# Kernel tuning notes

Measured on AMD Instinct MI355X. Metric: run time of the kernel, lower is better.

Reference implementation:

```python
import jax, jax.numpy as jnp
import numpy as np

DIM = 128; TIME_DIM = 256; HEADS = 8; WS = 4; GROUPS = 32
B = 8; H = 128; W = 128; EPS = 1e-5

def _rel_pos_index(ws):
    c = np.stack(np.meshgrid(np.arange(ws), np.arange(ws), indexing='ij')).reshape(2, -1)
    rel = (c[:, :, None] - c[:, None, :]).transpose(1, 2, 0)
    rel[:, :, 0] += ws - 1; rel[:, :, 1] += ws - 1
    rel[:, :, 0] *= 2 * ws - 1
    return jnp.asarray(rel.sum(-1))  # (ws*ws, ws*ws) int

REL_IDX = _rel_pos_index(WS)

def group_norm(x, w, b):
    Bx, C, Hx, Wx = x.shape
    xg = x.reshape(Bx, GROUPS, C // GROUPS, Hx, Wx)
    m = xg.mean((2, 3, 4), keepdims=True)
    v = xg.var((2, 3, 4), keepdims=True)
    x = ((xg - m) * jax.lax.rsqrt(v + EPS)).reshape(Bx, C, Hx, Wx)
    return x * w[None, :, None, None] + b[None, :, None, None]

def ada_gn(x, w, b, scale, shift):
    return group_norm(x, w, b) * (1.0 + scale[:, :, None, None]) + shift[:, :, None, None]

def time_mlp(t, w1, b1, w2, b2):
    h = jax.nn.silu(t @ w1.T + b1)
    out = h @ w2.T + b2
    scale, shift = jnp.split(out, 2, axis=-1)
    return scale, shift

def conv1x1(x, w, b):
    return jnp.einsum('bchw,oc->bohw', x, w) + b[None, :, None, None]

def window_attn(x, qkv_w, qkv_b, proj_w, proj_b, rel_bias):
    Bx, C, Hx, Wx = x.shape
    hd = C // HEADS
    nH, nW = Hx // WS, Wx // WS
    # partition into non-overlapping WSxWS windows -> (Nw, T, C)
    xw = x.transpose(0, 2, 3, 1).reshape(Bx, nH, WS, nW, WS, C)
    xw = xw.transpose(0, 1, 3, 2, 4, 5).reshape(Bx * nH * nW, WS * WS, C)
    qkv = xw @ qkv_w.T + qkv_b
    Nw, T, _ = qkv.shape
    qkv = qkv.reshape(Nw, T, 3, HEADS, hd).transpose(2, 0, 3, 1, 4)
    q, k, v = qkv[0], qkv[1], qkv[2]
    attn = jnp.einsum('whtd,whsd->whts', q, k) * (hd ** -0.5)
    bias = rel_bias[REL_IDX]  # (T, T, heads) gather from Swin rel-pos table
    attn = jax.nn.softmax(attn + bias.transpose(2, 0, 1)[None], axis=-1)
    out = jnp.einsum('whts,whsd->whtd', attn, v).transpose(0, 2, 1, 3).reshape(Nw, T, C)
    out = out @ proj_w.T + proj_b
    out = out.reshape(Bx, nH, nW, WS, WS, C).transpose(0, 1, 3, 2, 4, 5).reshape(Bx, Hx, Wx, C)
    return out.transpose(0, 3, 1, 2)

def reference(x, t_emb, gn1_w, gn1_b, t1_w1, t1_b1, t1_w2, t1_b2, spec_w, spec_b, mode_w,
              gn2_w, gn2_b, t2_w1, t2_b1, t2_w2, t2_b2, qkv_w, qkv_b, proj_w, proj_b, rel_bias,
              gn3_w, gn3_b, t3_w1, t3_b1, t3_w2, t3_b2, mlp_w1, mlp_b1, mlp_w2, mlp_b2,
              sb_gn_w, sb_gn_b, dw_w, dw_b, pw_w, pw_b):
    # --- AdaGN -> DCTSpectralConv -> SiLU -> residual ---
    s1, sh1 = time_mlp(t_emb, t1_w1, t1_b1, t1_w2, t1_b2)
    h = ada_gn(x, gn1_w, gn1_b, s1, sh1)
    h = h * jax.nn.sigmoid(mode_w)[None, :, None, None]  # per-mode weighting
    h = conv1x1(h, spec_w, spec_b)
    x = x + jax.nn.silu(h)
    # --- AdaGN -> windowed attention -> residual ---
    s2, sh2 = time_mlp(t_emb, t2_w1, t2_b1, t2_w2, t2_b2)
    h = ada_gn(x, gn2_w, gn2_b, s2, sh2)
    x = x + window_attn(h, qkv_w, qkv_b, proj_w, proj_b, rel_bias)
    # --- AdaGN -> ChannelMLP -> residual ---
    s3, sh3 = time_mlp(t_emb, t3_w1, t3_b1, t3_w2, t3_b2)
    h = ada_gn(x, gn3_w, gn3_b, s3, sh3)
    h = conv1x1(h, mlp_w1, mlp_b1)
    h = jax.nn.silu(h)
    h = conv1x1(h, mlp_w2, mlp_b2)
    x = x + h
    # --- SpatialBlock: GN -> depthwise 3x3 -> SiLU -> pointwise -> residual ---
    h = group_norm(x, sb_gn_w, sb_gn_b)
    h = jax.lax.conv_general_dilated(h, dw_w, (1, 1), 'SAME', feature_group_count=DIM,
                                     dimension_numbers=('NCHW', 'OIHW', 'NCHW'))
    h = h + dw_b[None, :, None, None]
    h = jax.nn.silu(h)
    h = conv1x1(h, pw_w, pw_b)
    return x + h


def setup_inputs() -> dict:
    key = jax.random.key(0)
    ks = jax.random.split(key, 24)
    r = lambda i, shape, s=1.0: jax.random.normal(ks[i], shape, dtype=jnp.float32) * s
    ones = lambda n: jnp.ones((n,), jnp.float32)
    zeros = lambda n: jnp.zeros((n,), jnp.float32)
    return {
        'x': r(0, (B, DIM, H, W)),
        't_emb': r(1, (B, TIME_DIM)),
        'gn1_w': ones(DIM), 'gn1_b': zeros(DIM),
        't1_w1': r(2, (DIM * 4, TIME_DIM), 0.02), 't1_b1': zeros(DIM * 4),
        't1_w2': r(3, (DIM * 2, DIM * 4), 0.02), 't1_b2': zeros(DIM * 2),
        'spec_w': r(4, (DIM, DIM), 0.05), 'spec_b': zeros(DIM),
        'mode_w': ones(DIM),
        'gn2_w': ones(DIM), 'gn2_b': zeros(DIM),
        't2_w1': r(5, (DIM * 4, TIME_DIM), 0.02), 't2_b1': zeros(DIM * 4),
        't2_w2': r(6, (DIM * 2, DIM * 4), 0.02), 't2_b2': zeros(DIM * 2),
        'qkv_w': r(7, (3 * DIM, DIM), 0.05), 'qkv_b': zeros(3 * DIM),
        'proj_w': r(8, (DIM, DIM), 0.05), 'proj_b': zeros(DIM),
        'rel_bias': r(9, ((2 * WS - 1) ** 2, HEADS), 0.02),
        'gn3_w': ones(DIM), 'gn3_b': zeros(DIM),
        't3_w1': r(10, (DIM * 4, TIME_DIM), 0.02), 't3_b1': zeros(DIM * 4),
        't3_w2': r(11, (DIM * 2, DIM * 4), 0.02), 't3_b2': zeros(DIM * 2),
        'mlp_w1': r(12, (DIM * 4, DIM), 0.05), 'mlp_b1': zeros(DIM * 4),
        'mlp_w2': r(13, (DIM, DIM * 4), 0.05), 'mlp_b2': zeros(DIM),
        'sb_gn_w': ones(DIM), 'sb_gn_b': zeros(DIM),
        'dw_w': r(14, (DIM, 1, 3, 3), 0.1), 'dw_b': zeros(DIM),
        'pw_w': r(15, (DIM, DIM), 0.05), 'pw_b': zeros(DIM),
    }
```

## Files before the change

### kernel.cpp

```cpp
#include <hip/hip_runtime.h>

#define PTOT 131072
#define IMGP 16384
#define BATCH 8
#define EPSV 1e-5f

typedef short bf16x8 __attribute__((ext_vector_type(8)));
typedef float f32x4 __attribute__((ext_vector_type(4)));

__device__ __forceinline__ float bf2f(unsigned short u){
  union { unsigned int i; float f; } v; v.i = ((unsigned int)u) << 16; return v.f;
}
__device__ __forceinline__ unsigned short f2bf(float f){
  union { float f; unsigned int i; } v; v.f = f;
  unsigned int r = v.i + 0x7FFFu + ((v.i >> 16) & 1u);
  return (unsigned short)(r >> 16);
}
__device__ __forceinline__ unsigned int pk2(float a, float b){
  return (unsigned int)f2bf(a) | ((unsigned int)f2bf(b) << 16);
}
__device__ __forceinline__ float sigmoidf_(float x){ return 1.f/(1.f + __expf(-x)); }

__device__ __forceinline__ void ld16bf(const unsigned short* p, float* f){
  uint4 u0 = *(const uint4*)p;
  uint4 u1 = *(const uint4*)(p+8);
  f[0]=bf2f((unsigned short)u0.x); f[1]=bf2f((unsigned short)(u0.x>>16));
  f[2]=bf2f((unsigned short)u0.y); f[3]=bf2f((unsigned short)(u0.y>>16));
  f[4]=bf2f((unsigned short)u0.z); f[5]=bf2f((unsigned short)(u0.z>>16));
  f[6]=bf2f((unsigned short)u0.w); f[7]=bf2f((unsigned short)(u0.w>>16));
  f[8]=bf2f((unsigned short)u1.x); f[9]=bf2f((unsigned short)(u1.x>>16));
  f[10]=bf2f((unsigned short)u1.y); f[11]=bf2f((unsigned short)(u1.y>>16));
  f[12]=bf2f((unsigned short)u1.z); f[13]=bf2f((unsigned short)(u1.z>>16));
  f[14]=bf2f((unsigned short)u1.w); f[15]=bf2f((unsigned short)(u1.w>>16));
}

__global__ __launch_bounds__(256) void k_prep(
    const float* __restrict__ a0, const float* __restrict__ a1,
    const float* __restrict__ a2, const float* __restrict__ a3,
    const float* __restrict__ a4, const float* __restrict__ a5,
    unsigned short* __restrict__ dst)
{
  int i = blockIdx.x*256 + threadIdx.x;
  if (i >= 229376) return;
  float v;
  if (i < 16384) v = a0[i];
  else if (i < 65536) v = a1[i-16384];
  else if (i < 81920) v = a2[i-65536];
  else if (i < 147456) v = a3[i-81920];
  else if (i < 212992) v = a4[i-147456];
  else v = a5[i-212992];
  dst[i] = f2bf(v);
}

__global__ __launch_bounds__(256) void k_time_mlp(
    const float* __restrict__ temb,
    const float* __restrict__ w1a, const float* __restrict__ b1a,
    const float* __restrict__ w2a, const float* __restrict__ b2a,
    const float* __restrict__ w1b, const float* __restrict__ b1b,
    const float* __restrict__ w2b, const float* __restrict__ b2b,
    const float* __restrict__ w1c, const float* __restrict__ b1c,
    const float* __restrict__ w2c, const float* __restrict__ b2c,
    float* __restrict__ scsh)
{
  int b = blockIdx.x, s = blockIdx.y, t = threadIdx.x;
  const float* w1 = (s==0)? w1a : ((s==1)? w1b : w1c);
  const float* b1 = (s==0)? b1a : ((s==1)? b1b : b1c);
  const float* w2 = (s==0)? w2a : ((s==1)? w2b : w2c);
  const float* b2 = (s==0)? b2a : ((s==1)? b2b : b2c);
  __shared__ float te[256];
  __shared__ float hb[512];
  te[t] = temb[b*256 + t];
  __syncthreads();
  for (int k = t; k < 512; k += 256){
    float acc = b1[k];
    const float* wr = w1 + (size_t)k*256;
    for (int j = 0; j < 256; j += 4){
      float4 w = *(const float4*)(wr + j);
      acc += w.x*te[j] + w.y*te[j+1] + w.z*te[j+2] + w.w*te[j+3];
    }
    hb[k] = acc * sigmoidf_(acc);
  }
  __syncthreads();
  {
    float acc = b2[t];
    const float* wr = w2 + (size_t)t*512;
    for (int j = 0; j < 512; j += 4){
      float4 w = *(const float4*)(wr + j);
      acc += w.x*hb[j] + w.y*hb[j+1] + w.z*hb[j+2] + w.w*hb[j+3];
    }
    scsh[(size_t)(s*BATCH + b)*256 + t] = acc;
  }
}

__global__ __launch_bounds__(256) void k_pre(
    const float* __restrict__ x0, float* __restrict__ X0T, float* __restrict__ SG1)
{
  __shared__ __align__(16) float T[64*136];
  __shared__ float sgS[32], sgSS[32];
  int t = threadIdx.x;
  int p0 = blockIdx.x << 6;
  int b = p0 >> 14;
  int win0 = (p0 >> 4) & 1023;
  int wh = win0 >> 5, ww0 = win0 & 31;
  if (t < 32){ sgS[t]=0.f; sgSS[t]=0.f; }
  int q = t & 3;
  int cb = t >> 2;
  #pragma unroll
  for (int ci = 0; ci < 2; ++ci){
    int c = cb + ci*64;
    const float* src = x0 + ((size_t)(b*128 + c))*IMGP + (wh*4)*128 + ww0*4 + q*4;
    #pragma unroll
    for (int ty = 0; ty < 4; ++ty){
      float4 v = *(const float4*)(src + ty*128);
      T[(q*16 + ty*4 + 0)*136 + c] = v.x;
      T[(q*16 + ty*4 + 1)*136 + c] = v.y;
      T[(q*16 + ty*4 + 2)*136 + c] = v.z;
      T[(q*16 + ty*4 + 3)*136 + c] = v.w;
    }
  }
  __syncthreads();
  {
    int px = t >> 2, c0 = (t & 3) << 5;
    float* dst = X0T + ((size_t)(p0+px))*128 + c0;
    const float* src = T + px*136 + c0;
    #pragma unroll
    for (int gi = 0; gi < 8; ++gi){
      float4 v = *(const float4*)(src + gi*4);
      *(float4*)(dst + gi*4) = v;
      atomicAdd(&sgS[(c0>>2)+gi],  v.x+v.y+v.z+v.w);
      atomicAdd(&sgSS[(c0>>2)+gi], v.x*v.x+v.y*v.y+v.z*v.z+v.w*v.w);
    }
  }
  __syncthreads();
  if (t < 32){
    atomicAdd(&SG1[(b*32+t)*2],   sgS[t]);
    atomicAdd(&SG1[(b*32+t)*2+1], sgSS[t]);
  }
}

__global__ __launch_bounds__(256) void k_s1(
    const float* __restrict__ X0T,
    const float* __restrict__ SG1, float* __restrict__ SG2,
    const unsigned short* __restrict__ Wbf, const float* __restrict__ bias,
    const float* __restrict__ gnw, const float* __restrict__ gnb,
    const float* __restrict__ scsh, const float* __restrict__ modew,
    float* __restrict__ XR)
{
  __shared__ __align__(16) unsigned short Bs[64*136];
  __shared__ __align__(16) char UN[64*136*4];
  __shared__ float An[128], Bn[128];
  __shared__ float sgS[32], sgSS[32];
  unsigned short* As = (unsigned short*)UN;
  float* OT = (float*)UN;
  int t = threadIdx.x;
  int p0 = blockIdx.x << 6;
  int b = p0 >> 14;
  if (t < 128){
    int g = t >> 2;
    float S = SG1[(b*32+g)*2], SS = SG1[(b*32+g)*2+1];
    float m = S*(1.f/65536.f);
    float r = rsqrtf(SS*(1.f/65536.f) - m*m + EPSV);
    float sc = 1.f + scsh[b*256 + t];
    float sh = scsh[b*256 + 128 + t];
    float a = r*gnw[t]*sc;
    float bb = (gnb[t] - m*r*gnw[t])*sc + sh;
    float sg = sigmoidf_(modew[t]); a *= sg; bb *= sg;
    An[t] = a; Bn[t] = bb;
  }
  if (t < 32){ sgS[t]=0.f; sgSS[t]=0.f; }
  __syncthreads();
  {
    int px = t >> 2, c0 = (t & 3) << 5;
    const float* src = X0T + ((size_t)(p0+px))*128 + c0;
    unsigned short* dst = Bs + px*136 + c0;
    #pragma unroll
    for (int j = 0; j < 4; ++j){
      float4 v0 = *(const float4*)(src + j*8);
      float4 v1 = *(const float4*)(src + j*8 + 4);
      int c = c0 + j*8;
      uint4 w;
      w.x = pk2(fmaf(v0.x,An[c+0],Bn[c+0]), fmaf(v0.y,An[c+1],Bn[c+1]));
      w.y = pk2(fmaf(v0.z,An[c+2],Bn[c+2]), fmaf(v0.w,An[c+3],Bn[c+3]));
      w.z = pk2(fmaf(v1.x,An[c+4],Bn[c+4]), fmaf(v1.y,An[c+5],Bn[c+5]));
      w.w = pk2(fmaf(v1.z,An[c+6],Bn[c+6]), fmaf(v1.w,An[c+7],Bn[c+7]));
      *(uint4*)(dst + j*8) = w;
    }
  }
  f32x4 acc[2][4];
  #pragma unroll
  for (int i=0;i<2;++i)
    #pragma unroll
    for (int j=0;j<4;++j){ f32x4 z={0.f,0.f,0.f,0.f}; acc[i][j]=z; }
  int lane = t & 63, wv = t >> 6, quad = lane >> 4, l15 = lane & 15;
  for (int kc = 0; kc < 2; ++kc){
    __syncthreads();
    {
      int o = t >> 1, k0 = (t & 1) << 5;
      const unsigned short* src = Wbf + o*128 + kc*64 + k0;
      unsigned short* dst = As + o*72 + k0;
      #pragma unroll
      for (int j = 0; j < 4; ++j) *(uint4*)(dst + j*8) = *(const uint4*)(src + j*8);
    }
    __syncthreads();
    #pragma unroll
    for (int s = 0; s < 2; ++s){
      bf16x8 af[2], bfv[4];
      #pragma unroll
      for (int i=0;i<2;++i) af[i] = *(const bf16x8*)(As + (wv*32 + i*16 + l15)*72 + s*32 + quad*8);
      #pragma unroll
      for (int j=0;j<4;++j) bfv[j] = *(const bf16x8*)(Bs + (j*16 + l15)*136 + kc*64 + s*32 + quad*8);
      #pragma unroll
      for (int i=0;i<2;++i)
        #pragma unroll
        for (int j=0;j<4;++j)
          acc[i][j] = __builtin_amdgcn_mfma_f32_16x16x32_bf16(af[i], bfv[j], acc[i][j], 0,0,0);
    }
  }
  __syncthreads();
  #pragma unroll
  for (int i = 0; i < 2; ++i){
    int o = wv*32 + i*16 + (quad<<2);
    float4 bv = *(const float4*)(bias + o);
    #pragma unroll
    for (int j = 0; j < 4; ++j){
      int px = j*16 + l15;
      float v0=acc[i][j][0]+bv.x, v1=acc[i][j][1]+bv.y, v2=acc[i][j][2]+bv.z, v3=acc[i][j][3]+bv.w;
      v0*=sigmoidf_(v0); v1*=sigmoidf_(v1); v2*=sigmoidf_(v2); v3*=sigmoidf_(v3);
      float4 rv = *(const float4*)(X0T + ((size_t)(p0+px))*128 + o);
      v0+=rv.x; v1+=rv.y; v2+=rv.z; v3+=rv.w;
      *(float4*)(OT + px*136 + o) = make_float4(v0,v1,v2,v3);
    }
  }
  __syncthreads();
  {
    int px = t >> 2, c0 = (t & 3) << 5;
    float* dst = XR + ((size_t)(p0+px))*128 + c0;
    const float* src = OT + px*136 + c0;
    #pragma unroll
    for (int gi = 0; gi < 8; ++gi){
      float4 v = *(const float4*)(src + gi*4);
      *(float4*)(dst + gi*4) = v;
      atomicAdd(&sgS[(c0>>2)+gi],  v.x+v.y+v.z+v.w);
      atomicAdd(&sgSS[(c0>>2)+gi], v.x*v.x+v.y*v.y+v.z*v.z+v.w*v.w);
    }
  }
  __syncthreads();
  if (t < 32){
    atomicAdd(&SG2[(b*32+t)*2],   sgS[t]);
    atomicAdd(&SG2[(b*32+t)*2+1], sgSS[t]);
  }
}

__global__ __launch_bounds__(256) void k_s2(
    float* __restrict__ XR,
    const float* __restrict__ SG2, float* __restrict__ SG3,
    const unsigned short* __restrict__ Wqkv, const float* __restrict__ bqkv,
    const unsigned short* __restrict__ Wproj, const float* __restrict__ bproj,
    const float* __restrict__ relb,
    const float* __restrict__ gnw, const float* __restrict__ gnb,
    const float* __restrict__ scsh)
{
  __shared__ __align__(16) unsigned short Bs[32*136];
  __shared__ __align__(16) unsigned short QB[32*136];
  __shared__ __align__(16) unsigned short KB[32*136];
  __shared__ __align__(16) unsigned short VB[32*136];
  __shared__ __align__(16) char UN[18432];
  __shared__ float An[128], Bn[128];
  __shared__ float relbs[392];
  __shared__ float sgS[32], sgSS[32];
  unsigned short* As = (unsigned short*)UN;
  float* OT = (float*)UN;
  int t = threadIdx.x;
  int p0 = blockIdx.x << 5;
  int b = p0 >> 14;
  if (t < 128){
    int g = t >> 2;
    float S = SG2[(b*32+g)*2], SS = SG2[(b*32+g)*2+1];
    float m = S*(1.f/65536.f);
    float r = rsqrtf(SS*(1.f/65536.f) - m*m + EPSV);
    float sc = 1.f + scsh[b*256 + t];
    float sh = scsh[b*256 + 128 + t];
    An[t] = r*gnw[t]*sc;
    Bn[t] = (gnb[t] - m*r*gnw[t])*sc + sh;
  }
  for (int j = t; j < 392; j += 256) relbs[j] = relb[j];
  if (t < 32){ sgS[t]=0.f; sgSS[t]=0.f; }
  __syncthreads();
  {
    int px = t >> 3, c0 = (t & 7) << 4;
    const float* src = XR + ((size_t)(p0+px))*128 + c0;
    unsigned short* dst = Bs + px*136 + c0;
    #pragma unroll
    for (int j = 0; j < 2; ++j){
      float4 v0 = *(const float4*)(src + j*8);
      float4 v1 = *(const float4*)(src + j*8 + 4);
      int c = c0 + j*8;
      uint4 w;
      w.x = pk2(fmaf(v0.x,An[c+0],Bn[c+0]), fmaf(v0.y,An[c+1],Bn[c+1]));
      w.y = pk2(fmaf(v0.z,An[c+2],Bn[c+2]), fmaf(v0.w,An[c+3],Bn[c+3]));
      w.z = pk2(fmaf(v1.x,An[c+4],Bn[c+4]), fmaf(v1.y,An[c+5],Bn[c+5]));
      w.w = pk2(fmaf(v1.z,An[c+6],Bn[c+6]), fmaf(v1.w,An[c+7],Bn[c+7]));
      *(uint4*)(dst + j*8) = w;
    }
  }
  int lane = t & 63, wv = t >> 6, quad = lane >> 4, l15 = lane & 15;
  unsigned short* bufs[3] = {QB, KB, VB};
  for (int s = 0; s < 3; ++s){
    f32x4 acc[2][2];
    #pragma unroll
    for (int i=0;i<2;++i)
      #pragma unroll
      for (int j=0;j<2;++j){ f32x4 z={0.f,0.f,0.f,0.f}; acc[i][j]=z; }
    for (int kc = 0; kc < 2; ++kc){
      __syncthreads();
      {
        int o = t >> 1, k0 = (t & 1) << 5;
        const unsigned short* src = Wqkv + (size_t)(s*128+o)*128 + kc*64 + k0;
        unsigned short* dst = As + o*72 + k0;
        #pragma unroll
        for (int j = 0; j < 4; ++j) *(uint4*)(dst + j*8) = *(const uint4*)(src + j*8);
      }
      __syncthreads();
      #pragma unroll
      for (int ks = 0; ks < 2; ++ks){
        bf16x8 af[2], bfv[2];
        #pragma unroll
        for (int i=0;i<2;++i) af[i] = *(const bf16x8*)(As + (wv*32 + i*16 + l15)*72 + ks*32 + quad*8);
        #pragma unroll
        for (int j=0;j<2;++j) bfv[j] = *(const bf16x8*)(Bs + (j*16 + l15)*136 + kc*64 + ks*32 + quad*8);
        #pragma unroll
        for (int i=0;i<2;++i)
          #pragma unroll
          for (int j=0;j<2;++j)
            acc[i][j] = __builtin_amdgcn_mfma_f32_16x16x32_bf16(af[i], bfv[j], acc[i][j], 0,0,0);
      }
    }
    unsigned short* dstb = bufs[s];
    #pragma unroll
    for (int i = 0; i < 2; ++i){
      int o = wv*32 + i*16 + (quad<<2);
      float4 bv = *(const float4*)(bqkv + s*128 + o);
      #pragma unroll
      for (int j = 0; j < 2; ++j){
        int px = j*16 + l15;
        *(unsigned int*)(dstb + px*136 + o)     = pk2(acc[i][j][0]+bv.x, acc[i][j][1]+bv.y);
        *(unsigned int*)(dstb + px*136 + o + 2) = pk2(acc[i][j][2]+bv.z, acc[i][j][3]+bv.w);
      }
    }
  }
  __syncthreads();
  {
    int win = t >> 7, head = (t >> 4) & 7, tq = t & 15;
    float qv[16];
    ld16bf(QB + (win*16+tq)*136 + head*16, qv);
    float pr[16]; float mx = -1e30f;
    int ty = tq >> 2, tx = tq & 3;
    #pragma unroll
    for (int s16 = 0; s16 < 16; ++s16){
      float kv[16];
      ld16bf(KB + (win*16+s16)*136 + head*16, kv);
      float dot = 0.f;
      #pragma unroll
      for (int d = 0; d < 16; ++d) dot = fmaf(qv[d], kv[d], dot);
      int idx = (ty-(s16>>2)+3)*7 + (tx-(s16&3)+3);
      pr[s16] = dot*0.25f + relbs[idx*8 + head];
      mx = fmaxf(mx, pr[s16]);
    }
    float sum = 0.f;
    #pragma unroll
    for (int s16 = 0; s16 < 16; ++s16){ pr[s16] = __expf(pr[s16]-mx); sum += pr[s16]; }
    float inv = 1.f/sum;
    #pragma unroll
    for (int s16 = 0; s16 < 16; ++s16) pr[s16] *= inv;
    __syncthreads();
    float ov[16];
    #pragma unroll
    for (int d = 0; d < 16; ++d) ov[d] = 0.f;
    #pragma unroll
    for (int s16 = 0; s16 < 16; ++s16){
      float vv[16];
      ld16bf(VB + (win*16+s16)*136 + head*16, vv);
      #pragma unroll
      for (int d = 0; d < 16; ++d) ov[d] = fmaf(pr[s16], vv[d], ov[d]);
    }
    unsigned short* dst = QB + (win*16+tq)*136 + head*16;
    uint4 w0, w1;
    w0.x = pk2(ov[0],ov[1]);   w0.y = pk2(ov[2],ov[3]);
    w0.z = pk2(ov[4],ov[5]);   w0.w = pk2(ov[6],ov[7]);
    w1.x = pk2(ov[8],ov[9]);   w1.y = pk2(ov[10],ov[11]);
    w1.z = pk2(ov[12],ov[13]); w1.w = pk2(ov[14],ov[15]);
    *(uint4*)dst = w0;
    *(uint4*)(dst+8) = w1;
  }
  f32x4 acc[2][2];
  #pragma unroll
  for (int i=0;i<2;++i)
    #pragma unroll
    for (int j=0;j<2;++j){ f32x4 z={0.f,0.f,0.f,0.f}; acc[i][j]=z; }
  for (int kc = 0; kc < 2; ++kc){
    __syncthreads();
    {
      int o = t >> 1, k0 = (t & 1) << 5;
      const unsigned short* src = Wproj + (size_t)o*128 + kc*64 + k0;
      unsigned short* dst = As + o*72 + k0;
      #pragma unroll
      for (int j = 0; j < 4; ++j) *(uint4*)(dst + j*8) = *(const uint4*)(src + j*8);
    }
    __syncthreads();
    #pragma unroll
    for (int ks = 0; ks < 2; ++ks){
      bf16x8 af[2], bfv[2];
      #pragma unroll
      for (int i=0;i<2;++i) af[i] = *(const bf16x8*)(As + (wv*32 + i*16 + l15)*72 + ks*32 + quad*8);
      #pragma unroll
      for (int j=0;j<2;++j) bfv[j] = *(const bf16x8*)(QB + (j*16 + l15)*136 + kc*64 + ks*32 + quad*8);
      #pragma unroll
      for (int i=0;i<2;++i)
        #pragma unroll
        for (int j=0;j<2;++j)
          acc[i][j] = __builtin_amdgcn_mfma_f32_16x16x32_bf16(af[i], bfv[j], acc[i][j], 0,0,0);
    }
  }
  __syncthreads();
  #pragma unroll
  for (int i = 0; i < 2; ++i){
    int o = wv*32 + i*16 + (quad<<2);
    float4 bv = *(const float4*)(bproj + o);
    #pragma unroll
    for (int j = 0; j < 2; ++j){
      int px = j*16 + l15;
      float v0=acc[i][j][0]+bv.x, v1=acc[i][j][1]+bv.y, v2=acc[i][j][2]+bv.z, v3=acc[i][j][3]+bv.w;
      float4 rv = *(const float4*)(XR + ((size_t)(p0+px))*128 + o);
      v0+=rv.x; v1+=rv.y; v2+=rv.z; v3+=rv.w;
      *(float4*)(OT + px*136 + o) = make_float4(v0,v1,v2,v3);
    }
  }
  __syncthreads();
  {
    int px = t >> 3, c0 = (t & 7) << 4;
    float* dst = XR + ((size_t)(p0+px))*128 + c0;
    const float* src = OT + px*136 + c0;
    #pragma unroll
    for (int gi = 0; gi < 4; ++gi){
      float4 v = *(const float4*)(src + gi*4);
      *(float4*)(dst + gi*4) = v;
      atomicAdd(&sgS[(c0>>2)+gi],  v.x+v.y+v.z+v.w);
      atomicAdd(&sgSS[(c0>>2)+gi], v.x*v.x+v.y*v.y+v.z*v.z+v.w*v.w);
    }
  }
  __syncthreads();
  if (t < 32){
    atomicAdd(&SG3[(b*32+t)*2],   sgS[t]);
    atomicAdd(&SG3[(b*32+t)*2+1], sgSS[t]);
  }
}

__global__ __launch_bounds__(256) void k_s3(
    float* __restrict__ XR,
    const float* __restrict__ SG3, float* __restrict__ SG4,
    const unsigned short* __restrict__ W1, const float* __restrict__ b1,
    const unsigned short* __restrict__ W2, const float* __restrict__ b2,
    const float* __restrict__ gnw, const float* __restrict__ gnb,
    const float* __restrict__ scsh)
{
  __shared__ __align__(16) unsigned short Xs[64*136];
  __shared__ __align__(16) char UN[45056];
  __shared__ float An[128], Bn[128];
  __shared__ float sgS[32], sgSS[32];
  unsigned short* As1 = (unsigned short*)UN;
  unsigned short* Hs  = (unsigned short*)(UN + 17408);
  unsigned short* As2 = (unsigned short*)(UN + 26624);
  float* OT = (float*)UN;
  int t = threadIdx.x;
  int p0 = blockIdx.x << 6;
  int b = p0 >> 14;
  if (t < 128){
    int g = t >> 2;
    float S = SG3[(b*32+g)*2], SS = SG3[(b*32+g)*2+1];
    float m = S*(1.f/65536.f);
    float r = rsqrtf(SS*(1.f/65536.f) - m*m + EPSV);
    float sc = 1.f + scsh[b*256 + t];
    float sh = scsh[b*256 + 128 + t];
    An[t] = r*gnw[t]*sc;
    Bn[t] = (gnb[t] - m*r*gnw[t])*sc + sh;
  }
  if (t < 32){ sgS[t]=0.f; sgSS[t]=0.f; }
  __syncthreads();
  {
    int px = t >> 2, c0 = (t & 3) << 5;
    const float* src = XR + ((size_t)(p0+px))*128 + c0;
    unsigned short* dst = Xs + px*136 + c0;
    #pragma unroll
    for (int j = 0; j < 4; ++j){
      float4 v0 = *(const float4*)(src + j*8);
      float4 v1 = *(const float4*)(src + j*8 + 4);
      int c = c0 + j*8;
      uint4 w;
      w.x = pk2(fmaf(v0.x,An[c+0],Bn[c+0]), fmaf(v0.y,An[c+1],Bn[c+1]));
      w.y = pk2(fmaf(v0.z,An[c+2],Bn[c+2]), fmaf(v0.w,An[c+3],Bn[c+3]));
      w.z = pk2(fmaf(v1.x,An[c+4],Bn[c+4]), fmaf(v1.y,An[c+5],Bn[c+5]));
      w.w = pk2(fmaf(v1.z,An[c+6],Bn[c+6]), fmaf(v1.w,An[c+7],Bn[c+7]));
      *(uint4*)(dst + j*8) = w;
    }
  }
  int lane = t & 63, wv = t >> 6, quad = lane >> 4, l15 = lane & 15;
  f32x4 acc2[2][4];
  #pragma unroll
  for (int i=0;i<2;++i)
    #pragma unroll
    for (int j=0;j<4;++j){ f32x4 z={0.f,0.f,0.f,0.f}; acc2[i][j]=z; }
  for (int hc = 0; hc < 8; ++hc){
    __syncthreads();
    {
      int hr = t >> 2, k0 = (t & 3) << 5;
      const unsigned short* src = W1 + (size_t)(hc*64+hr)*128 + k0;
      unsigned short* dst = As1 + hr*136 + k0;
      #pragma unroll
      for (int j = 0; j < 4; ++j) *(uint4*)(dst + j*8) = *(const uint4*)(src + j*8);
    }
    {
      int o = t >> 1, k0 = (t & 1) << 5;
      const unsigned short* src = W2 + (size_t)o*512 + hc*64 + k0;
      unsigned short* dst = As2 + o*72 + k0;
      #pragma unroll
      for (int j = 0; j < 4; ++j) *(uint4*)(dst + j*8) = *(const uint4*)(src + j*8);
    }
    __syncthreads();
    {
      int hb = (wv & 1) << 5, pxb = (wv >> 1) << 5;
      f32x4 a1[2][2];
      #pragma unroll
      for (int i=0;i<2;++i)
        #pragma unroll
        for (int j=0;j<2;++j){ f32x4 z={0.f,0.f,0.f,0.f}; a1[i][j]=z; }
      #pragma unroll
      for (int s = 0; s < 4; ++s){
        bf16x8 af[2], bfv[2];
        #pragma unroll
        for (int i=0;i<2;++i) af[i] = *(const bf16x8*)(As1 + (hb + i*16 + l15)*136 + s*32 + quad*8);
        #pragma unroll
        for (int j=0;j<2;++j) bfv[j] = *(const bf16x8*)(Xs + (pxb + j*16 + l15)*136 + s*32 + quad*8);
        #pragma unroll
        for (int i=0;i<2;++i)
          #pragma unroll
          for (int j=0;j<2;++j)
            a1[i][j] = __builtin_amdgcn_mfma_f32_16x16x32_bf16(af[i], bfv[j], a1[i][j], 0,0,0);
      }
      #pragma unroll
      for (int i = 0; i < 2; ++i){
        int hl = hb + i*16 + (quad<<2);
        float4 bv = *(const float4*)(b1 + hc*64 + hl);
        #pragma unroll
        for (int j = 0; j < 2; ++j){
          int px = pxb + j*16 + l15;
          float v0=a1[i][j][0]+bv.x, v1=a1[i][j][1]+bv.y, v2=a1[i][j][2]+bv.z, v3=a1[i][j][3]+bv.w;
          v0*=sigmoidf_(v0); v1*=sigmoidf_(v1); v2*=sigmoidf_(v2); v3*=sigmoidf_(v3);
          *(unsigned int*)(Hs + px*72 + hl)     = pk2(v0, v1);
          *(unsigned int*)(Hs + px*72 + hl + 2) = pk2(v2, v3);
        }
      }
    }
    __syncthreads();
    {
      int ob = wv << 5;
      #pragma unroll
      for (int s = 0; s < 2; ++s){
        bf16x8 af[2], bfv[4];
        #pragma unroll
        for (int i=0;i<2;++i) af[i] = *(const bf16x8*)(As2 + (ob + i*16 + l15)*72 + s*32 + quad*8);
        #pragma unroll
        for (int j=0;j<4;++j) bfv[j] = *(const bf16x8*)(Hs + (j*16 + l15)*72 + s*32 + quad*8);
        #pragma unroll
        for (int i=0;i<2;++i)
          #pragma unroll
          for (int j=0;j<4;++j)
            acc2[i][j] = __builtin_amdgcn_mfma_f32_16x16x32_bf16(af[i], bfv[j], acc2[i][j], 0,0,0);
      }
    }
  }
  __syncthreads();
  #pragma unroll
  for (int i = 0; i < 2; ++i){
    int o = (wv<<5) + i*16 + (quad<<2);
    float4 bv = *(const float4*)(b2 + o);
    #pragma unroll
    for (int j = 0; j < 4; ++j){
      int px = j*16 + l15;
      float v0=acc2[i][j][0]+bv.x, v1=acc2[i][j][1]+bv.y, v2=acc2[i][j][2]+bv.z, v3=acc2[i][j][3]+bv.w;
      float4 rv = *(const float4*)(XR + ((size_t)(p0+px))*128 + o);
      v0+=rv.x; v1+=rv.y; v2+=rv.z; v3+=rv.w;
      *(float4*)(OT + px*136 + o) = make_float4(v0,v1,v2,v3);
    }
  }
  __syncthreads();
  {
    int px = t >> 2, c0 = (t & 3) << 5;
    float* dst = XR + ((size_t)(p0+px))*128 + c0;
    const float* src = OT + px*136 + c0;
    #pragma unroll
    for (int gi = 0; gi < 8; ++gi){
      float4 v = *(const float4*)(src + gi*4);
      *(float4*)(dst + gi*4) = v;
      atomicAdd(&sgS[(c0>>2)+gi],  v.x+v.y+v.z+v.w);
      atomicAdd(&sgSS[(c0>>2)+gi], v.x*v.x+v.y*v.y+v.z*v.z+v.w*v.w);
    }
  }
  __syncthreads();
  if (t < 32){
    atomicAdd(&SG4[(b*32+t)*2],   sgS[t]);
    atomicAdd(&SG4[(b*32+t)*2+1], sgSS[t]);
  }
}

__global__ __launch_bounds__(256) void k_dw(
    const float* __restrict__ XR, const float* __restrict__ SG4,
    const float* __restrict__ gnw, const float* __restrict__ gnb,
    const float* __restrict__ dww, const float* __restrict__ dwb,
    unsigned short* __restrict__ DWO)
{
  __shared__ float wt[9*128];
  __shared__ float An[128], Bn[128];
  int t = threadIdx.x;
  int p0 = blockIdx.x << 6;
  int b = p0 >> 14;
  int win0 = (p0 >> 4) & 1023;
  int wh = win0 >> 5, ww0 = win0 & 31;
  if (t < 128){
    int g = t >> 2;
    float S = SG4[(b*32+g)*2], SS = SG4[(b*32+g)*2+1];
    float m = S*(1.f/65536.f);
    float r = rsqrtf(SS*(1.f/65536.f) - m*m + EPSV);
    float A = r*gnw[t];
    An[t] = A;
    Bn[t] = gnb[t] - m*A;
  }
  for (int j = t; j < 1152; j += 256){ int c = j/9, tap = j%9; wt[tap*128 + c] = dww[j]; }
  __syncthreads();
  int pxl = t & 63, ck = t >> 6;
  int c0 = ck << 5;
  int wloc = pxl >> 4, ty = (pxl >> 2) & 3, tx = pxl & 3;
  int h = wh*4 + ty, w = (ww0 + wloc)*4 + tx;
  float acc[32];
  #pragma unroll
  for (int j = 0; j < 8; ++j){
    float4 bv = *(const float4*)(dwb + c0 + j*4);
    acc[j*4+0]=bv.x; acc[j*4+1]=bv.y; acc[j*4+2]=bv.z; acc[j*4+3]=bv.w;
  }
  #pragma unroll
  for (int dy = -1; dy <= 1; ++dy){
    int hh = h + dy;
    if (hh < 0 || hh > 127) continue;
    #pragma unroll
    for (int dx = -1; dx <= 1; ++dx){
      int wn = w + dx;
      if (wn < 0 || wn > 127) continue;
      int pn = b*IMGP + ((hh>>2)*32 + (wn>>2))*16 + (hh&3)*4 + (wn&3);
      const float* xp = XR + (size_t)pn*128 + c0;
      const float* wp = wt + ((dy+1)*3 + (dx+1))*128 + c0;
      #pragma unroll
      for (int j = 0; j < 8; ++j){
        float4 xv = *(const float4*)(xp + j*4);
        float4 wv = *(const float4*)(wp + j*4);
        int c = c0 + j*4;
        acc[j*4+0] = fmaf(wv.x, fmaf(An[c+0], xv.x, Bn[c+0]), acc[j*4+0]);
        acc[j*4+1] = fmaf(wv.y, fmaf(An[c+1], xv.y, Bn[c+1]), acc[j*4+1]);
        acc[j*4+2] = fmaf(wv.z, fmaf(An[c+2], xv.z, Bn[c+2]), acc[j*4+2]);
        acc[j*4+3] = fmaf(wv.w, fmaf(An[c+3], xv.w, Bn[c+3]), acc[j*4+3]);
      }
    }
  }
  unsigned short* dst = DWO + ((size_t)(p0+pxl))*128 + c0;
  #pragma unroll
  for (int j = 0; j < 4; ++j){
    float v0 = acc[j*8+0], v1 = acc[j*8+1], v2 = acc[j*8+2], v3 = acc[j*8+3];
    float v4 = acc[j*8+4], v5 = acc[j*8+5], v6 = acc[j*8+6], v7 = acc[j*8+7];
    v0*=sigmoidf_(v0); v1*=sigmoidf_(v1); v2*=sigmoidf_(v2); v3*=sigmoidf_(v3);
    v4*=sigmoidf_(v4); v5*=sigmoidf_(v5); v6*=sigmoidf_(v6); v7*=sigmoidf_(v7);
    uint4 wq;
    wq.x = pk2(v0,v1); wq.y = pk2(v2,v3); wq.z = pk2(v4,v5); wq.w = pk2(v6,v7);
    *(uint4*)(dst + j*8) = wq;
  }
}

__global__ __launch_bounds__(256) void k_s4(
    const unsigned short* __restrict__ DWO,
    const unsigned short* __restrict__ Wbf, const float* __restrict__ bias,
    const float* __restrict__ XR, float* __restrict__ out)
{
  __shared__ __align__(16) unsigned short Bs[64*136];
  __shared__ __align__(16) char UN[64*136*4];
  unsigned short* As = (unsigned short*)UN;
  float* OT = (float*)UN;
  int t = threadIdx.x;
  int p0 = blockIdx.x << 6;
  int b = p0 >> 14;
  int win0 = (p0 >> 4) & 1023;
  int wh = win0 >> 5, ww0 = win0 & 31;
  {
    int px = t >> 2, c0 = (t & 3) << 5;
    const unsigned short* src = DWO + ((size_t)(p0+px))*128 + c0;
    unsigned short* dst = Bs + px*136 + c0;
    #pragma unroll
    for (int j = 0; j < 4; ++j) *(uint4*)(dst + j*8) = *(const uint4*)(src + j*8);
  }
  f32x4 acc[2][4];
  #pragma unroll
  for (int i=0;i<2;++i)
    #pragma unroll
    for (int j=0;j<4;++j){ f32x4 z={0.f,0.f,0.f,0.f}; acc[i][j]=z; }
  int lane = t & 63, wv = t >> 6, quad = lane >> 4, l15 = lane & 15;
  for (int kc = 0; kc < 2; ++kc){
    __syncthreads();
    {
      int o = t >> 1, k0 = (t & 1) << 5;
      const unsigned short* src = Wbf + (size_t)o*128 + kc*64 + k0;
      unsigned short* dst = As + o*72 + k0;
      #pragma unroll
      for (int j = 0; j < 4; ++j) *(uint4*)(dst + j*8) = *(const uint4*)(src + j*8);
    }
    __syncthreads();
    #pragma unroll
    for (int s = 0; s < 2; ++s){
      bf16x8 af[2], bfv[4];
      #pragma unroll
      for (int i=0;i<2;++i) af[i] = *(const bf16x8*)(As + (wv*32 + i*16 + l15)*72 + s*32 + quad*8);
      #pragma unroll
      for (int j=0;j<4;++j) bfv[j] = *(const bf16x8*)(Bs + (j*16 + l15)*136 + kc*64 + s*32 + quad*8);
      #pragma unroll
      for (int i=0;i<2;++i)
        #pragma unroll
        for (int j=0;j<4;++j)
          acc[i][j] = __builtin_amdgcn_mfma_f32_16x16x32_bf16(af[i], bfv[j], acc[i][j], 0,0,0);
    }
  }
  __syncthreads();
  #pragma unroll
  for (int i = 0; i < 2; ++i){
    int o = (wv<<5) + i*16 + (quad<<2);
    float4 bv = *(const float4*)(bias + o);
    #pragma unroll
    for (int j = 0; j < 4; ++j){
      int px = j*16 + l15;
      float v0=acc[i][j][0]+bv.x, v1=acc[i][j][1]+bv.y, v2=acc[i][j][2]+bv.z, v3=acc[i][j][3]+bv.w;
      float4 rv = *(const float4*)(XR + ((size_t)(p0+px))*128 + o);
      v0+=rv.x; v1+=rv.y; v2+=rv.z; v3+=rv.w;
      *(float4*)(OT + px*136 + o) = make_float4(v0,v1,v2,v3);
    }
  }
  __syncthreads();
  #pragma unroll
  for (int it = 0; it < 2; ++it){
    int item = t + (it << 8);
    int c = item >> 2, ty = item & 3;
    float vbuf[16];
    #pragma unroll
    for (int wl = 0; wl < 4; ++wl)
      #pragma unroll
      for (int tx = 0; tx < 4; ++tx)
        vbuf[wl*4+tx] = OT[(wl*16 + ty*4 + tx)*136 + c];
    float* dst = out + ((size_t)(b*128 + c))*IMGP + (wh*4+ty)*128 + ww0*4;
    #pragma unroll
    for (int j = 0; j < 4; ++j)
      *(float4*)(dst + j*4) = make_float4(vbuf[j*4], vbuf[j*4+1], vbuf[j*4+2], vbuf[j*4+3]);
  }
}

extern "C" void kernel_launch(void* const* d_in, const int* in_sizes, int n_in,
                              void* d_out, int out_size, void* d_ws, size_t ws_size,
                              hipStream_t stream)
{
  const float* x0   = (const float*)d_in[0];
  const float* temb = (const float*)d_in[1];
  const float* gn1w = (const float*)d_in[2];
  const float* gn1b = (const float*)d_in[3];
  const float* t1w1 = (const float*)d_in[4];
  const float* t1b1 = (const float*)d_in[5];
  const float* t1w2 = (const float*)d_in[6];
  const float* t1b2 = (const float*)d_in[7];
  const float* specw= (const float*)d_in[8];
  const float* specb= (const float*)d_in[9];
  const float* modew= (const float*)d_in[10];
  const float* gn2w = (const float*)d_in[11];
  const float* gn2b = (const float*)d_in[12];
  const float* t2w1 = (const float*)d_in[13];
  const float* t2b1 = (const float*)d_in[14];
  const float* t2w2 = (const float*)d_in[15];
  const float* t2b2 = (const float*)d_in[16];
  const float* qkvw = (const float*)d_in[17];
  const float* qkvb = (const float*)d_in[18];
  const float* projw= (const float*)d_in[19];
  const float* projb= (const float*)d_in[20];
  const float* relb = (const float*)d_in[21];
  const float* gn3w = (const float*)d_in[22];
  const float* gn3b = (const float*)d_in[23];
  const float* t3w1 = (const float*)d_in[24];
  const float* t3b1 = (const float*)d_in[25];
  const float* t3w2 = (const float*)d_in[26];
  const float* t3b2 = (const float*)d_in[27];
  const float* mlpw1= (const float*)d_in[28];
  const float* mlpb1= (const float*)d_in[29];
  const float* mlpw2= (const float*)d_in[30];
  const float* mlpb2= (const float*)d_in[31];
  const float* sbgnw= (const float*)d_in[32];
  const float* sbgnb= (const float*)d_in[33];
  const float* dww  = (const float*)d_in[34];
  const float* dwb  = (const float*)d_in[35];
  const float* pww  = (const float*)d_in[36];
  const float* pwb  = (const float*)d_in[37];
  float* out = (float*)d_out;

  char* ws = (char*)d_ws;
  float* SC  = (float*)ws;
  float* SG  = (float*)(ws + 32768);
  float* SG1 = SG, *SG2 = SG+512, *SG3 = SG+1024, *SG4 = SG+1536;
  unsigned short* WBF = (unsigned short*)(ws + 65536);
  unsigned short* Wspec = WBF;
  unsigned short* Wqkv  = WBF + 16384;
  unsigned short* Wproj = WBF + 65536;
  unsigned short* Wmlp1 = WBF + 81920;
  unsigned short* Wmlp2 = WBF + 147456;
  unsigned short* Wpw   = WBF + 212992;
  float* X0T = (float*)(ws + (1u<<20));
  float* XR  = (float*)(ws + (1u<<20) + ((size_t)64<<20));
  unsigned short* DWO = (unsigned short*)(ws + (1u<<20) + ((size_t)128<<20));

  hipMemsetAsync(SG, 0, 4*512*sizeof(float), stream);

  k_prep<<<896, 256, 0, stream>>>(specw, qkvw, projw, mlpw1, mlpw2, pww, WBF);
  k_time_mlp<<<dim3(8,3), 256, 0, stream>>>(temb,
      t1w1,t1b1,t1w2,t1b2, t2w1,t2b1,t2w2,t2b2, t3w1,t3b1,t3w2,t3b2, SC);
  k_pre<<<2048, 256, 0, stream>>>(x0, X0T, SG1);
  k_s1<<<2048, 256, 0, stream>>>(X0T, SG1, SG2, Wspec, specb,
      gn1w, gn1b, SC + 0, modew, XR);
  k_s2<<<4096, 256, 0, stream>>>(XR, SG2, SG3, Wqkv, qkvb, Wproj, projb,
      relb, gn2w, gn2b, SC + 2048);
  k_s3<<<2048, 256, 0, stream>>>(XR, SG3, SG4, Wmlp1, mlpb1, Wmlp2, mlpb2,
      gn3w, gn3b, SC + 4096);
  k_dw<<<2048, 256, 0, stream>>>(XR, SG4, sbgnw, sbgnb, dww, dwb, DWO);
  k_s4<<<2048, 256, 0, stream>>>(DWO, Wpw, pwb, XR, out);
}
```

Baseline: 810.5 us.

## Store intermediates in bf16, split attention into QKV GEMM and attention-proj kernels

Intermediate activations (transposed input, residual stream, depthwise output) are now stored as bf16 instead of fp32, which halves global memory traffic between stages. The combined window-attention kernel is split into a separate QKV GEMM kernel and an attention-plus-projection kernel that works on spatial strips. The GEMM tiles grow to 128 pixels per block with a 4x4 MFMA tile per wave. Pixel ordering changes from window-major to row-major, so the final output store is coalesced. The cost is lower precision in the residual stream and an extra QKV round trip through global memory.

```diff
diff --git a/kernel.cpp b/kernel.cpp
--- a/kernel.cpp
+++ b/kernel.cpp
@@ -1,6 +1,5 @@
 #include <hip/hip_runtime.h>
 
-#define PTOT 131072
 #define IMGP 16384
 #define BATCH 8
 #define EPSV 1e-5f
@@ -21,17 +20,19 @@
 }
 __device__ __forceinline__ float sigmoidf_(float x){ return 1.f/(1.f + __expf(-x)); }
 
-__device__ __forceinline__ void ld16bf(const unsigned short* p, float* f){
-  uint4 u0 = *(const uint4*)p;
-  uint4 u1 = *(const uint4*)(p+8);
-  f[0]=bf2f((unsigned short)u0.x); f[1]=bf2f((unsigned short)(u0.x>>16));
-  f[2]=bf2f((unsigned short)u0.y); f[3]=bf2f((unsigned short)(u0.y>>16));
-  f[4]=bf2f((unsigned short)u0.z); f[5]=bf2f((unsigned short)(u0.z>>16));
-  f[6]=bf2f((unsigned short)u0.w); f[7]=bf2f((unsigned short)(u0.w>>16));
-  f[8]=bf2f((unsigned short)u1.x); f[9]=bf2f((unsigned short)(u1.x>>16));
-  f[10]=bf2f((unsigned short)u1.y); f[11]=bf2f((unsigned short)(u1.y>>16));
-  f[12]=bf2f((unsigned short)u1.z); f[13]=bf2f((unsigned short)(u1.z>>16));
-  f[14]=bf2f((unsigned short)u1.w); f[15]=bf2f((unsigned short)(u1.w>>16));
+__device__ __forceinline__ void ub8(uint4 u, float* f){
+  f[0]=bf2f((unsigned short)(u.x&0xffff)); f[1]=bf2f((unsigned short)(u.x>>16));
+  f[2]=bf2f((unsigned short)(u.y&0xffff)); f[3]=bf2f((unsigned short)(u.y>>16));
+  f[4]=bf2f((unsigned short)(u.z&0xffff)); f[5]=bf2f((unsigned short)(u.z>>16));
+  f[6]=bf2f((unsigned short)(u.w&0xffff)); f[7]=bf2f((unsigned short)(u.w>>16));
+}
+__device__ __forceinline__ uint4 pb8(const float* f){
+  uint4 r; r.x = pk2(f[0],f[1]); r.y = pk2(f[2],f[3]);
+  r.z = pk2(f[4],f[5]); r.w = pk2(f[6],f[7]); return r;
+}
+__device__ __forceinline__ void ld16lds(const unsigned short* p, float* f){
+  uint4 u0 = *(const uint4*)p; uint4 u1 = *(const uint4*)(p+8);
+  ub8(u0, f); ub8(u1, f+8);
 }
 
 __global__ __launch_bounds__(256) void k_prep(
@@ -52,7 +53,7 @@
   dst[i] = f2bf(v);
 }
 
-__global__ __launch_bounds__(256) void k_time_mlp(
+__global__ __launch_bounds__(256) void k_tmlp(
     const float* __restrict__ temb,
     const float* __restrict__ w1a, const float* __restrict__ b1a,
     const float* __restrict__ w2a, const float* __restrict__ b2a,
@@ -93,43 +94,41 @@
 }
 
 __global__ __launch_bounds__(256) void k_pre(
-    const float* __restrict__ x0, float* __restrict__ X0T, float* __restrict__ SG1)
-{
-  __shared__ __align__(16) float T[64*136];
+    const float* __restrict__ x0, unsigned short* __restrict__ X0b, float* __restrict__ SG1)
+{
+  __shared__ __align__(16) unsigned short T[64*136];
   __shared__ float sgS[32], sgSS[32];
   int t = threadIdx.x;
   int p0 = blockIdx.x << 6;
   int b = p0 >> 14;
-  int win0 = (p0 >> 4) & 1023;
-  int wh = win0 >> 5, ww0 = win0 & 31;
+  int hw0 = p0 & 16383;
   if (t < 32){ sgS[t]=0.f; sgSS[t]=0.f; }
-  int q = t & 3;
-  int cb = t >> 2;
-  #pragma unroll
-  for (int ci = 0; ci < 2; ++ci){
-    int c = cb + ci*64;
-    const float* src = x0 + ((size_t)(b*128 + c))*IMGP + (wh*4)*128 + ww0*4 + q*4;
-    #pragma unroll
-    for (int ty = 0; ty < 4; ++ty){
-      float4 v = *(const float4*)(src + ty*128);
-      T[(q*16 + ty*4 + 0)*136 + c] = v.x;
-      T[(q*16 + ty*4 + 1)*136 + c] = v.y;
-      T[(q*16 + ty*4 + 2)*136 + c] = v.z;
-      T[(q*16 + ty*4 + 3)*136 + c] = v.w;
-    }
+  __syncthreads();
+  {
+    int c = t >> 1, q = t & 1;
+    const float* src = x0 + (size_t)(b*128 + c)*IMGP + hw0 + q*32;
+    float s = 0.f, ss = 0.f;
+    #pragma unroll
+    for (int i = 0; i < 8; ++i){
+      float4 v = *(const float4*)(src + i*4);
+      int px = q*32 + i*4;
+      T[(px+0)*136 + c] = f2bf(v.x);
+      T[(px+1)*136 + c] = f2bf(v.y);
+      T[(px+2)*136 + c] = f2bf(v.z);
+      T[(px+3)*136 + c] = f2bf(v.w);
+      s  += v.x + v.y + v.z + v.w;
+      ss += v.x*v.x + v.y*v.y + v.z*v.z + v.w*v.w;
+    }
+    atomicAdd(&sgS[c>>2], s);
+    atomicAdd(&sgSS[c>>2], ss);
   }
   __syncthreads();
   {
     int px = t >> 2, c0 = (t & 3) << 5;
-    float* dst = X0T + ((size_t)(p0+px))*128 + c0;
-    const float* src = T + px*136 + c0;
-    #pragma unroll
-    for (int gi = 0; gi < 8; ++gi){
-      float4 v = *(const float4*)(src + gi*4);
-      *(float4*)(dst + gi*4) = v;
-      atomicAdd(&sgS[(c0>>2)+gi],  v.x+v.y+v.z+v.w);
-      atomicAdd(&sgSS[(c0>>2)+gi], v.x*v.x+v.y*v.y+v.z*v.z+v.w*v.w);
-    }
+    unsigned short* dst = X0b + (size_t)(p0+px)*128 + c0;
+    const unsigned short* srcT = T + px*136 + c0;
+    #pragma unroll
+    for (int g = 0; g < 4; ++g) *(uint4*)(dst + g*8) = *(const uint4*)(srcT + g*8);
   }
   __syncthreads();
   if (t < 32){
@@ -139,21 +138,21 @@
 }
 
 __global__ __launch_bounds__(256) void k_s1(
-    const float* __restrict__ X0T,
+    const unsigned short* __restrict__ X0b,
     const float* __restrict__ SG1, float* __restrict__ SG2,
     const unsigned short* __restrict__ Wbf, const float* __restrict__ bias,
     const float* __restrict__ gnw, const float* __restrict__ gnb,
     const float* __restrict__ scsh, const float* __restrict__ modew,
-    float* __restrict__ XR)
-{
-  __shared__ __align__(16) unsigned short Bs[64*136];
-  __shared__ __align__(16) char UN[64*136*4];
+    unsigned short* __restrict__ XRb)
+{
+  __shared__ __align__(16) char UN[36864];
   __shared__ float An[128], Bn[128];
   __shared__ float sgS[32], sgSS[32];
   unsigned short* As = (unsigned short*)UN;
-  float* OT = (float*)UN;
+  unsigned short* Bs = (unsigned short*)(UN + 18432);
+  unsigned short* OT = (unsigned short*)UN;
   int t = threadIdx.x;
-  int p0 = blockIdx.x << 6;
+  int p0 = blockIdx.x << 7;
   int b = p0 >> 14;
   if (t < 128){
     int g = t >> 2;
@@ -169,48 +168,45 @@
   }
   if (t < 32){ sgS[t]=0.f; sgSS[t]=0.f; }
   __syncthreads();
-  {
-    int px = t >> 2, c0 = (t & 3) << 5;
-    const float* src = X0T + ((size_t)(p0+px))*128 + c0;
-    unsigned short* dst = Bs + px*136 + c0;
-    #pragma unroll
-    for (int j = 0; j < 4; ++j){
-      float4 v0 = *(const float4*)(src + j*8);
-      float4 v1 = *(const float4*)(src + j*8 + 4);
-      int c = c0 + j*8;
-      uint4 w;
-      w.x = pk2(fmaf(v0.x,An[c+0],Bn[c+0]), fmaf(v0.y,An[c+1],Bn[c+1]));
-      w.y = pk2(fmaf(v0.z,An[c+2],Bn[c+2]), fmaf(v0.w,An[c+3],Bn[c+3]));
-      w.z = pk2(fmaf(v1.x,An[c+4],Bn[c+4]), fmaf(v1.y,An[c+5],Bn[c+5]));
-      w.w = pk2(fmaf(v1.z,An[c+6],Bn[c+6]), fmaf(v1.w,An[c+7],Bn[c+7]));
-      *(uint4*)(dst + j*8) = w;
-    }
-  }
-  f32x4 acc[2][4];
-  #pragma unroll
-  for (int i=0;i<2;++i)
+  int lane = t & 63, wv = t >> 6, quad = lane >> 4, l15 = lane & 15;
+  int wo = (wv & 1) << 6, wp = (wv >> 1) << 6;
+  f32x4 acc[4][4];
+  #pragma unroll
+  for (int i=0;i<4;++i)
     #pragma unroll
     for (int j=0;j<4;++j){ f32x4 z={0.f,0.f,0.f,0.f}; acc[i][j]=z; }
-  int lane = t & 63, wv = t >> 6, quad = lane >> 4, l15 = lane & 15;
   for (int kc = 0; kc < 2; ++kc){
-    __syncthreads();
-    {
-      int o = t >> 1, k0 = (t & 1) << 5;
-      const unsigned short* src = Wbf + o*128 + kc*64 + k0;
-      unsigned short* dst = As + o*72 + k0;
+    if (kc) __syncthreads();
+    { int o = t >> 1, kh = (t & 1) << 5;
+      const unsigned short* src = Wbf + o*128 + kc*64 + kh;
+      unsigned short* dst = As + o*72 + kh;
       #pragma unroll
       for (int j = 0; j < 4; ++j) *(uint4*)(dst + j*8) = *(const uint4*)(src + j*8);
     }
+    { int px = t >> 1, kh = (t & 1) << 5;
+      const unsigned short* src = X0b + (size_t)(p0+px)*128 + kc*64 + kh;
+      unsigned short* dst = Bs + px*72 + kh;
+      #pragma unroll
+      for (int j = 0; j < 4; ++j){
+        uint4 u = *(const uint4*)(src + j*8);
+        float f[8], g[8];
+        ub8(u, f);
+        int c = kc*64 + kh + j*8;
+        #pragma unroll
+        for (int e = 0; e < 8; ++e) g[e] = fmaf(f[e], An[c+e], Bn[c+e]);
+        *(uint4*)(dst + j*8) = pb8(g);
+      }
+    }
     __syncthreads();
     #pragma unroll
     for (int s = 0; s < 2; ++s){
-      bf16x8 af[2], bfv[4];
-      #pragma unroll
-      for (int i=0;i<2;++i) af[i] = *(const bf16x8*)(As + (wv*32 + i*16 + l15)*72 + s*32 + quad*8);
-      #pragma unroll
-      for (int j=0;j<4;++j) bfv[j] = *(const bf16x8*)(Bs + (j*16 + l15)*136 + kc*64 + s*32 + quad*8);
-      #pragma unroll
-      for (int i=0;i<2;++i)
+      bf16x8 af[4], bfv[4];
+      #pragma unroll
+      for (int i=0;i<4;++i) af[i]  = *(const bf16x8*)(As + (wo+i*16+l15)*72 + s*32 + quad*8);
+      #pragma unroll
+      for (int j=0;j<4;++j) bfv[j] = *(const bf16x8*)(Bs + (wp+j*16+l15)*72 + s*32 + quad*8);
+      #pragma unroll
+      for (int i=0;i<4;++i)
         #pragma unroll
         for (int j=0;j<4;++j)
           acc[i][j] = __builtin_amdgcn_mfma_f32_16x16x32_bf16(af[i], bfv[j], acc[i][j], 0,0,0);
@@ -218,30 +214,38 @@
   }
   __syncthreads();
   #pragma unroll
-  for (int i = 0; i < 2; ++i){
-    int o = wv*32 + i*16 + (quad<<2);
+  for (int i = 0; i < 4; ++i){
+    int o = wo + i*16 + (quad<<2);
     float4 bv = *(const float4*)(bias + o);
     #pragma unroll
     for (int j = 0; j < 4; ++j){
-      int px = j*16 + l15;
+      int px = wp + j*16 + l15;
       float v0=acc[i][j][0]+bv.x, v1=acc[i][j][1]+bv.y, v2=acc[i][j][2]+bv.z, v3=acc[i][j][3]+bv.w;
       v0*=sigmoidf_(v0); v1*=sigmoidf_(v1); v2*=sigmoidf_(v2); v3*=sigmoidf_(v3);
-      float4 rv = *(const float4*)(X0T + ((size_t)(p0+px))*128 + o);
-      v0+=rv.x; v1+=rv.y; v2+=rv.z; v3+=rv.w;
-      *(float4*)(OT + px*136 + o) = make_float4(v0,v1,v2,v3);
+      uint2 w; w.x = pk2(v0,v1); w.y = pk2(v2,v3);
+      *(uint2*)(OT + px*136 + o) = w;
     }
   }
   __syncthreads();
   {
-    int px = t >> 2, c0 = (t & 3) << 5;
-    float* dst = XR + ((size_t)(p0+px))*128 + c0;
-    const float* src = OT + px*136 + c0;
-    #pragma unroll
-    for (int gi = 0; gi < 8; ++gi){
-      float4 v = *(const float4*)(src + gi*4);
-      *(float4*)(dst + gi*4) = v;
-      atomicAdd(&sgS[(c0>>2)+gi],  v.x+v.y+v.z+v.w);
-      atomicAdd(&sgSS[(c0>>2)+gi], v.x*v.x+v.y*v.y+v.z*v.z+v.w*v.w);
+    int px = t >> 1, c0 = (t & 1) << 6;
+    const unsigned short* rsrc = X0b + (size_t)(p0+px)*128 + c0;
+    unsigned short* dst = XRb + (size_t)(p0+px)*128 + c0;
+    #pragma unroll
+    for (int g = 0; g < 8; ++g){
+      uint4 hu = *(const uint4*)(OT + px*136 + c0 + g*8);
+      uint4 ru = *(const uint4*)(rsrc + g*8);
+      float hf[8], rf[8], v[8];
+      ub8(hu, hf); ub8(ru, rf);
+      #pragma unroll
+      for (int e = 0; e < 8; ++e) v[e] = hf[e] + rf[e];
+      float slo = v[0]+v[1]+v[2]+v[3], shi = v[4]+v[5]+v[6]+v[7];
+      float qlo = v[0]*v[0]+v[1]*v[1]+v[2]*v[2]+v[3]*v[3];
+      float qhi = v[4]*v[4]+v[5]*v[5]+v[6]*v[6]+v[7]*v[7];
+      int gb = (c0 + g*8) >> 2;
+      atomicAdd(&sgS[gb], slo);  atomicAdd(&sgS[gb+1], shi);
+      atomicAdd(&sgSS[gb], qlo); atomicAdd(&sgSS[gb+1], qhi);
+      *(uint4*)(dst + g*8) = pb8(v);
     }
   }
   __syncthreads();
@@ -251,28 +255,23 @@
   }
 }
 
-__global__ __launch_bounds__(256) void k_s2(
-    float* __restrict__ XR,
-    const float* __restrict__ SG2, float* __restrict__ SG3,
-    const unsigned short* __restrict__ Wqkv, const float* __restrict__ bqkv,
-    const unsigned short* __restrict__ Wproj, const float* __restrict__ bproj,
-    const float* __restrict__ relb,
+__global__ __launch_bounds__(256) void k_qkv(
+    const unsigned short* __restrict__ XRb,
+    const float* __restrict__ SG2,
+    const unsigned short* __restrict__ Wq, const float* __restrict__ bq,
     const float* __restrict__ gnw, const float* __restrict__ gnb,
-    const float* __restrict__ scsh)
-{
-  __shared__ __align__(16) unsigned short Bs[32*136];
-  __shared__ __align__(16) unsigned short QB[32*136];
-  __shared__ __align__(16) unsigned short KB[32*136];
-  __shared__ __align__(16) unsigned short VB[32*136];
-  __shared__ __align__(16) char UN[18432];
+    const float* __restrict__ scsh,
+    unsigned short* __restrict__ QKV)
+{
+  __shared__ __align__(16) char UN[36864];
   __shared__ float An[128], Bn[128];
-  __shared__ float relbs[392];
-  __shared__ float sgS[32], sgSS[32];
   unsigned short* As = (unsigned short*)UN;
-  float* OT = (float*)UN;
+  unsigned short* Bs = (unsigned short*)(UN + 18432);
+  unsigned short* OT = (unsigned short*)UN;
   int t = threadIdx.x;
-  int p0 = blockIdx.x << 5;
+  int p0 = blockIdx.x << 7;
   int b = p0 >> 14;
+  int sel = blockIdx.y;
   if (t < 128){
     int g = t >> 2;
     float S = SG2[(b*32+g)*2], SS = SG2[(b*32+g)*2+1];
@@ -283,169 +282,216 @@
     An[t] = r*gnw[t]*sc;
     Bn[t] = (gnb[t] - m*r*gnw[t])*sc + sh;
   }
+  __syncthreads();
+  int lane = t & 63, wv = t >> 6, quad = lane >> 4, l15 = lane & 15;
+  int wo = (wv & 1) << 6, wp = (wv >> 1) << 6;
+  f32x4 acc[4][4];
+  #pragma unroll
+  for (int i=0;i<4;++i)
+    #pragma unroll
+    for (int j=0;j<4;++j){ f32x4 z={0.f,0.f,0.f,0.f}; acc[i][j]=z; }
+  for (int kc = 0; kc < 2; ++kc){
+    if (kc) __syncthreads();
+    { int o = t >> 1, kh = (t & 1) << 5;
+      const unsigned short* src = Wq + (size_t)sel*16384 + o*128 + kc*64 + kh;
+      unsigned short* dst = As + o*72 + kh;
+      #pragma unroll
+      for (int j = 0; j < 4; ++j) *(uint4*)(dst + j*8) = *(const uint4*)(src + j*8);
+    }
+    { int px = t >> 1, kh = (t & 1) << 5;
+      const unsigned short* src = XRb + (size_t)(p0+px)*128 + kc*64 + kh;
+      unsigned short* dst = Bs + px*72 + kh;
+      #pragma unroll
+      for (int j = 0; j < 4; ++j){
+        uint4 u = *(const uint4*)(src + j*8);
+        float f[8], g[8];
+        ub8(u, f);
+        int c = kc*64 + kh + j*8;
+        #pragma unroll
+        for (int e = 0; e < 8; ++e) g[e] = fmaf(f[e], An[c+e], Bn[c+e]);
+        *(uint4*)(dst + j*8) = pb8(g);
+      }
+    }
+    __syncthreads();
+    #pragma unroll
+    for (int s = 0; s < 2; ++s){
+      bf16x8 af[4], bfv[4];
+      #pragma unroll
+      for (int i=0;i<4;++i) af[i]  = *(const bf16x8*)(As + (wo+i*16+l15)*72 + s*32 + quad*8);
+      #pragma unroll
+      for (int j=0;j<4;++j) bfv[j] = *(const bf16x8*)(Bs + (wp+j*16+l15)*72 + s*32 + quad*8);
+      #pragma unroll
+      for (int i=0;i<4;++i)
+        #pragma unroll
+        for (int j=0;j<4;++j)
+          acc[i][j] = __builtin_amdgcn_mfma_f32_16x16x32_bf16(af[i], bfv[j], acc[i][j], 0,0,0);
+    }
+  }
+  __syncthreads();
+  #pragma unroll
+  for (int i = 0; i < 4; ++i){
+    int o = wo + i*16 + (quad<<2);
+    float4 bv = *(const float4*)(bq + sel*128 + o);
+    #pragma unroll
+    for (int j = 0; j < 4; ++j){
+      int px = wp + j*16 + l15;
+      uint2 w; w.x = pk2(acc[i][j][0]+bv.x, acc[i][j][1]+bv.y);
+      w.y = pk2(acc[i][j][2]+bv.z, acc[i][j][3]+bv.w);
+      *(uint2*)(OT + px*136 + o) = w;
+    }
+  }
+  __syncthreads();
+  {
+    int px = t >> 1, og = (t & 1) << 6;
+    unsigned short* dst = QKV + (size_t)(p0+px)*384 + (sel << 7) + og;
+    const unsigned short* src = OT + px*136 + og;
+    #pragma unroll
+    for (int g = 0; g < 8; ++g) *(uint4*)(dst + g*8) = *(const uint4*)(src + g*8);
+  }
+}
+
+__global__ __launch_bounds__(256) void k_ap(
+    const unsigned short* __restrict__ QKV,
+    const unsigned short* __restrict__ Wproj, const float* __restrict__ bproj,
+    const float* __restrict__ relb,
+    unsigned short* __restrict__ XRb, float* __restrict__ SG3)
+{
+  __shared__ __align__(16) unsigned short AOb[128*136];
+  __shared__ __align__(16) unsigned short UNQ[12288];
+  __shared__ float relbs[392];
+  __shared__ float sgS[32], sgSS[32];
+  unsigned short* QKVs = UNQ;
+  unsigned short* As = UNQ;
+  int t = threadIdx.x;
+  int blk = blockIdx.x;
+  int b = blk >> 7;
+  int rem = blk & 127;
+  int h0 = (rem >> 2) << 2;
+  int w0 = (rem & 3) << 5;
+  int baseP = b*IMGP + h0*128 + w0;
   for (int j = t; j < 392; j += 256) relbs[j] = relb[j];
   if (t < 32){ sgS[t]=0.f; sgSS[t]=0.f; }
+  for (int hb = 0; hb < 8; hb += 2){
+    __syncthreads();
+    #pragma unroll
+    for (int pass = 0; pass < 6; ++pass){
+      int u = t + (pass << 8);
+      int sel = u >> 9;
+      int r = u & 511;
+      int hp = r >> 8;
+      int pxh = r & 255;
+      int pxl = pxh >> 1;
+      int dh = (pxh & 1) << 3;
+      int pg = baseP + ((pxl >> 5) << 7) + (pxl & 31);
+      *(uint4*)(QKVs + (((sel*2+hp) << 7) + pxl)*16 + dh) =
+        *(const uint4*)(QKV + (size_t)pg*384 + (sel << 7) + ((hb+hp) << 4) + dh);
+    }
+    __syncthreads();
+    {
+      int hp = t >> 7, win = (t >> 4) & 7, tq = t & 15;
+      int head = hb + hp;
+      int ty = tq >> 2, tx = tq & 3;
+      int pq = (ty << 5) + (win << 2) + tx;
+      float qv[16];
+      ld16lds(QKVs + ((hp << 7) + pq)*16, qv);
+      float pr[16]; float mx = -1e30f;
+      #pragma unroll
+      for (int s = 0; s < 16; ++s){
+        int ps = ((s >> 2) << 5) + (win << 2) + (s & 3);
+        float kv[16];
+        ld16lds(QKVs + (((2+hp) << 7) + ps)*16, kv);
+        float dot = 0.f;
+        #pragma unroll
+        for (int d = 0; d < 16; ++d) dot = fmaf(qv[d], kv[d], dot);
+        int idx = (ty-(s>>2)+3)*7 + (tx-(s&3)+3);
+        pr[s] = dot*0.25f + relbs[idx*8 + head];
+        mx = fmaxf(mx, pr[s]);
+      }
+      float sum = 0.f;
+      #pragma unroll
+      for (int s = 0; s < 16; ++s){ pr[s] = __expf(pr[s]-mx); sum += pr[s]; }
+      float inv = 1.f/sum;
+      float ov[16];
+      #pragma unroll
+      for (int d = 0; d < 16; ++d) ov[d] = 0.f;
+      #pragma unroll
+      for (int s = 0; s < 16; ++s){
+        int ps = ((s >> 2) << 5) + (win << 2) + (s & 3);
+        float vv[16];
+        ld16lds(QKVs + (((4+hp) << 7) + ps)*16, vv);
+        #pragma unroll
+        for (int d = 0; d < 16; ++d) ov[d] = fmaf(pr[s], vv[d], ov[d]);
+      }
+      #pragma unroll
+      for (int d = 0; d < 16; ++d) ov[d] *= inv;
+      unsigned short* dst = AOb + pq*136 + (head << 4);
+      *(uint4*)dst     = pb8(ov);
+      *(uint4*)(dst+8) = pb8(ov+8);
+    }
+  }
+  int lane = t & 63, wv = t >> 6, quad = lane >> 4, l15 = lane & 15;
+  int wo = (wv & 1) << 6, wp = (wv >> 1) << 6;
+  f32x4 acc[4][4];
+  #pragma unroll
+  for (int i=0;i<4;++i)
+    #pragma unroll
+    for (int j=0;j<4;++j){ f32x4 z={0.f,0.f,0.f,0.f}; acc[i][j]=z; }
+  for (int kc = 0; kc < 2; ++kc){
+    __syncthreads();
+    { int o = t >> 1, kh = (t & 1) << 5;
+      const unsigned short* src = Wproj + o*128 + kc*64 + kh;
+      unsigned short* dst = As + o*72 + kh;
+      #pragma unroll
+      for (int j = 0; j < 4; ++j) *(uint4*)(dst + j*8) = *(const uint4*)(src + j*8);
+    }
+    __syncthreads();
+    #pragma unroll
+    for (int s = 0; s < 2; ++s){
+      bf16x8 af[4], bfv[4];
+      #pragma unroll
+      for (int i=0;i<4;++i) af[i]  = *(const bf16x8*)(As + (wo+i*16+l15)*72 + s*32 + quad*8);
+      #pragma unroll
+      for (int j=0;j<4;++j) bfv[j] = *(const bf16x8*)(AOb + (wp+j*16+l15)*136 + kc*64 + s*32 + quad*8);
+      #pragma unroll
+      for (int i=0;i<4;++i)
+        #pragma unroll
+        for (int j=0;j<4;++j)
+          acc[i][j] = __builtin_amdgcn_mfma_f32_16x16x32_bf16(af[i], bfv[j], acc[i][j], 0,0,0);
+    }
+  }
+  __syncthreads();
+  #pragma unroll
+  for (int i = 0; i < 4; ++i){
+    int o = wo + i*16 + (quad<<2);
+    float4 bv = *(const float4*)(bproj + o);
+    #pragma unroll
+    for (int j = 0; j < 4; ++j){
+      int px = wp + j*16 + l15;
+      uint2 w; w.x = pk2(acc[i][j][0]+bv.x, acc[i][j][1]+bv.y);
+      w.y = pk2(acc[i][j][2]+bv.z, acc[i][j][3]+bv.w);
+      *(uint2*)(AOb + px*136 + o) = w;
+    }
+  }
   __syncthreads();
   {
-    int px = t >> 3, c0 = (t & 7) << 4;
-    const float* src = XR + ((size_t)(p0+px))*128 + c0;
-    unsigned short* dst = Bs + px*136 + c0;
-    #pragma unroll
-    for (int j = 0; j < 2; ++j){
-      float4 v0 = *(const float4*)(src + j*8);
-      float4 v1 = *(const float4*)(src + j*8 + 4);
-      int c = c0 + j*8;
-      uint4 w;
-      w.x = pk2(fmaf(v0.x,An[c+0],Bn[c+0]), fmaf(v0.y,An[c+1],Bn[c+1]));
-      w.y = pk2(fmaf(v0.z,An[c+2],Bn[c+2]), fmaf(v0.w,An[c+3],Bn[c+3]));
-      w.z = pk2(fmaf(v1.x,An[c+4],Bn[c+4]), fmaf(v1.y,An[c+5],Bn[c+5]));
-      w.w = pk2(fmaf(v1.z,An[c+6],Bn[c+6]), fmaf(v1.w,An[c+7],Bn[c+7]));
-      *(uint4*)(dst + j*8) = w;
-    }
-  }
-  int lane = t & 63, wv = t >> 6, quad = lane >> 4, l15 = lane & 15;
-  unsigned short* bufs[3] = {QB, KB, VB};
-  for (int s = 0; s < 3; ++s){
-    f32x4 acc[2][2];
-    #pragma unroll
-    for (int i=0;i<2;++i)
-      #pragma unroll
-      for (int j=0;j<2;++j){ f32x4 z={0.f,0.f,0.f,0.f}; acc[i][j]=z; }
-    for (int kc = 0; kc < 2; ++kc){
-      __syncthreads();
-      {
-        int o = t >> 1, k0 = (t & 1) << 5;
-        const unsigned short* src = Wqkv + (size_t)(s*128+o)*128 + kc*64 + k0;
-        unsigned short* dst = As + o*72 + k0;
-        #pragma unroll
-        for (int j = 0; j < 4; ++j) *(uint4*)(dst + j*8) = *(const uint4*)(src + j*8);
-      }
-      __syncthreads();
-      #pragma unroll
-      for (int ks = 0; ks < 2; ++ks){
-        bf16x8 af[2], bfv[2];
-        #pragma unroll
-        for (int i=0;i<2;++i) af[i] = *(const bf16x8*)(As + (wv*32 + i*16 + l15)*72 + ks*32 + quad*8);
-        #pragma unroll
-        for (int j=0;j<2;++j) bfv[j] = *(const bf16x8*)(Bs + (j*16 + l15)*136 + kc*64 + ks*32 + quad*8);
-        #pragma unroll
-        for (int i=0;i<2;++i)
-          #pragma unroll
-          for (int j=0;j<2;++j)
-            acc[i][j] = __builtin_amdgcn_mfma_f32_16x16x32_bf16(af[i], bfv[j], acc[i][j], 0,0,0);
-      }
-    }
-    unsigned short* dstb = bufs[s];
-    #pragma unroll
-    for (int i = 0; i < 2; ++i){
-      int o = wv*32 + i*16 + (quad<<2);
-      float4 bv = *(const float4*)(bqkv + s*128 + o);
-      #pragma unroll
-      for (int j = 0; j < 2; ++j){
-        int px = j*16 + l15;
-        *(unsigned int*)(dstb + px*136 + o)     = pk2(acc[i][j][0]+bv.x, acc[i][j][1]+bv.y);
-        *(unsigned int*)(dstb + px*136 + o + 2) = pk2(acc[i][j][2]+bv.z, acc[i][j][3]+bv.w);
-      }
-    }
-  }
-  __syncthreads();
-  {
-    int win = t >> 7, head = (t >> 4) & 7, tq = t & 15;
-    float qv[16];
-    ld16bf(QB + (win*16+tq)*136 + head*16, qv);
-    float pr[16]; float mx = -1e30f;
-    int ty = tq >> 2, tx = tq & 3;
-    #pragma unroll
-    for (int s16 = 0; s16 < 16; ++s16){
-      float kv[16];
-      ld16bf(KB + (win*16+s16)*136 + head*16, kv);
-      float dot = 0.f;
-      #pragma unroll
-      for (int d = 0; d < 16; ++d) dot = fmaf(qv[d], kv[d], dot);
-      int idx = (ty-(s16>>2)+3)*7 + (tx-(s16&3)+3);
-      pr[s16] = dot*0.25f + relbs[idx*8 + head];
-      mx = fmaxf(mx, pr[s16]);
-    }
-    float sum = 0.f;
-    #pragma unroll
-    for (int s16 = 0; s16 < 16; ++s16){ pr[s16] = __expf(pr[s16]-mx); sum += pr[s16]; }
-    float inv = 1.f/sum;
-    #pragma unroll
-    for (int s16 = 0; s16 < 16; ++s16) pr[s16] *= inv;
-    __syncthreads();
-    float ov[16];
-    #pragma unroll
-    for (int d = 0; d < 16; ++d) ov[d] = 0.f;
-    #pragma unroll
-    for (int s16 = 0; s16 < 16; ++s16){
-      float vv[16];
-      ld16bf(VB + (win*16+s16)*136 + head*16, vv);
-      #pragma unroll
-      for (int d = 0; d < 16; ++d) ov[d] = fmaf(pr[s16], vv[d], ov[d]);
-    }
-    unsigned short* dst = QB + (win*16+tq)*136 + head*16;
-    uint4 w0, w1;
-    w0.x = pk2(ov[0],ov[1]);   w0.y = pk2(ov[2],ov[3]);
-    w0.z = pk2(ov[4],ov[5]);   w0.w = pk2(ov[6],ov[7]);
-    w1.x = pk2(ov[8],ov[9]);   w1.y = pk2(ov[10],ov[11]);
-    w1.z = pk2(ov[12],ov[13]); w1.w = pk2(ov[14],ov[15]);
-    *(uint4*)dst = w0;
-    *(uint4*)(dst+8) = w1;
-  }
-  f32x4 acc[2][2];
-  #pragma unroll
-  for (int i=0;i<2;++i)
-    #pragma unroll
-    for (int j=0;j<2;++j){ f32x4 z={0.f,0.f,0.f,0.f}; acc[i][j]=z; }
-  for (int kc = 0; kc < 2; ++kc){
-    __syncthreads();
-    {
-      int o = t >> 1, k0 = (t & 1) << 5;
-      const unsigned short* src = Wproj + (size_t)o*128 + kc*64 + k0;
-      unsigned short* dst = As + o*72 + k0;
-      #pragma unroll
-      for (int j = 0; j < 4; ++j) *(uint4*)(dst + j*8) = *(const uint4*)(src + j*8);
-    }
-    __syncthreads();
-    #pragma unroll
-    for (int ks = 0; ks < 2; ++ks){
-      bf16x8 af[2], bfv[2];
-      #pragma unroll
-      for (int i=0;i<2;++i) af[i] = *(const bf16x8*)(As + (wv*32 + i*16 + l15)*72 + ks*32 + quad*8);
-      #pragma unroll
-      for (int j=0;j<2;++j) bfv[j] = *(const bf16x8*)(QB + (j*16 + l15)*136 + kc*64 + ks*32 + quad*8);
-      #pragma unroll
-      for (int i=0;i<2;++i)
-        #pragma unroll
-        for (int j=0;j<2;++j)
-          acc[i][j] = __builtin_amdgcn_mfma_f32_16x16x32_bf16(af[i], bfv[j], acc[i][j], 0,0,0);
-    }
-  }
-  __syncthreads();
-  #pragma unroll
-  for (int i = 0; i < 2; ++i){
-    int o = wv*32 + i*16 + (quad<<2);
-    float4 bv = *(const float4*)(bproj + o);
-    #pragma unroll
-    for (int j = 0; j < 2; ++j){
-      int px = j*16 + l15;
-      float v0=acc[i][j][0]+bv.x, v1=acc[i][j][1]+bv.y, v2=acc[i][j][2]+bv.z, v3=acc[i][j][3]+bv.w;
-      float4 rv = *(const float4*)(XR + ((size_t)(p0+px))*128 + o);
-      v0+=rv.x; v1+=rv.y; v2+=rv.z; v3+=rv.w;
-      *(float4*)(OT + px*136 + o) = make_float4(v0,v1,v2,v3);
-    }
-  }
-  __syncthreads();
-  {
-    int px = t >> 3, c0 = (t & 7) << 4;
-    float* dst = XR + ((size_t)(p0+px))*128 + c0;
-    const float* src = OT + px*136 + c0;
-    #pragma unroll
-    for (int gi = 0; gi < 4; ++gi){
-      float4 v = *(const float4*)(src + gi*4);
-      *(float4*)(dst + gi*4) = v;
-      atomicAdd(&sgS[(c0>>2)+gi],  v.x+v.y+v.z+v.w);
-      atomicAdd(&sgSS[(c0>>2)+gi], v.x*v.x+v.y*v.y+v.z*v.z+v.w*v.w);
+    int px = t >> 1, c0 = (t & 1) << 6;
+    int pg = baseP + ((px >> 5) << 7) + (px & 31);
+    unsigned short* dst = XRb + (size_t)pg*128 + c0;
+    #pragma unroll
+    for (int g = 0; g < 8; ++g){
+      uint4 hu = *(const uint4*)(AOb + px*136 + c0 + g*8);
+      uint4 ru = *(const uint4*)(dst + g*8);
+      float hf[8], rf[8], v[8];
+      ub8(hu, hf); ub8(ru, rf);
+      #pragma unroll
+      for (int e = 0; e < 8; ++e) v[e] = hf[e] + rf[e];
+      float slo = v[0]+v[1]+v[2]+v[3], shi = v[4]+v[5]+v[6]+v[7];
+      float qlo = v[0]*v[0]+v[1]*v[1]+v[2]*v[2]+v[3]*v[3];
+      float qhi = v[4]*v[4]+v[5]*v[5]+v[6]*v[6]+v[7]*v[7];
+      int gb = (c0 + g*8) >> 2;
+      atomicAdd(&sgS[gb], slo);  atomicAdd(&sgS[gb+1], shi);
+      atomicAdd(&sgSS[gb], qlo); atomicAdd(&sgSS[gb+1], qhi);
+      *(uint4*)(dst + g*8) = pb8(v);
     }
   }
   __syncthreads();
@@ -456,7 +502,7 @@
 }
 
 __global__ __launch_bounds__(256) void k_s3(
-    float* __restrict__ XR,
+    unsigned short* __restrict__ XRb,
     const float* __restrict__ SG3, float* __restrict__ SG4,
     const unsigned short* __restrict__ W1, const float* __restrict__ b1,
     const unsigned short* __restrict__ W2, const float* __restrict__ b2,
@@ -470,7 +516,7 @@
   unsigned short* As1 = (unsigned short*)UN;
   unsigned short* Hs  = (unsigned short*)(UN + 17408);
   unsigned short* As2 = (unsigned short*)(UN + 26624);
-  float* OT = (float*)UN;
+  unsigned short* OT  = (unsigned short*)UN;
   int t = threadIdx.x;
   int p0 = blockIdx.x << 6;
   int b = p0 >> 14;
@@ -487,23 +533,22 @@
   if (t < 32){ sgS[t]=0.f; sgSS[t]=0.f; }
   __syncthreads();
   {
-    int px = t >> 2, c0 = (t & 3) << 5;
-    const float* src = XR + ((size_t)(p0+px))*128 + c0;
-    unsigned short* dst = Xs + px*136 + c0;
+    int px = t >> 2, kh = (t & 3) << 5;
+    const unsigned short* src = XRb + (size_t)(p0+px)*128 + kh;
+    unsigned short* dst = Xs + px*136 + kh;
     #pragma unroll
     for (int j = 0; j < 4; ++j){
-      float4 v0 = *(const float4*)(src + j*8);
-      float4 v1 = *(const float4*)(src + j*8 + 4);
-      int c = c0 + j*8;
-      uint4 w;
-      w.x = pk2(fmaf(v0.x,An[c+0],Bn[c+0]), fmaf(v0.y,An[c+1],Bn[c+1]));
-      w.y = pk2(fmaf(v0.z,An[c+2],Bn[c+2]), fmaf(v0.w,An[c+3],Bn[c+3]));
-      w.z = pk2(fmaf(v1.x,An[c+4],Bn[c+4]), fmaf(v1.y,An[c+5],Bn[c+5]));
-      w.w = pk2(fmaf(v1.z,An[c+6],Bn[c+6]), fmaf(v1.w,An[c+7],Bn[c+7]));
-      *(uint4*)(dst + j*8) = w;
+      uint4 u = *(const uint4*)(src + j*8);
+      float f[8], g[8];
+      ub8(u, f);
+      int c = kh + j*8;
+      #pragma unroll
+      for (int e = 0; e < 8; ++e) g[e] = fmaf(f[e], An[c+e], Bn[c+e]);
+      *(uint4*)(dst + j*8) = pb8(g);
     }
   }
   int lane = t & 63, wv = t >> 6, quad = lane >> 4, l15 = lane & 15;
+  int hbv = (wv & 1) << 5, pxb = (wv >> 1) << 5, ob2 = wv << 5;
   f32x4 acc2[2][4];
   #pragma unroll
   for (int i=0;i<2;++i)
@@ -511,23 +556,20 @@
     for (int j=0;j<4;++j){ f32x4 z={0.f,0.f,0.f,0.f}; acc2[i][j]=z; }
   for (int hc = 0; hc < 8; ++hc){
     __syncthreads();
+    { int hr = t >> 2, kh = (t & 3) << 5;
+      const unsigned short* src = W1 + (size_t)(hc*64+hr)*128 + kh;
+      unsigned short* dst = As1 + hr*136 + kh;
+      #pragma unroll
+      for (int j = 0; j < 4; ++j) *(uint4*)(dst + j*8) = *(const uint4*)(src + j*8);
+    }
+    { int o = t >> 1, kh = (t & 1) << 5;
+      const unsigned short* src = W2 + (size_t)o*512 + hc*64 + kh;
+      unsigned short* dst = As2 + o*72 + kh;
+      #pragma unroll
+      for (int j = 0; j < 4; ++j) *(uint4*)(dst + j*8) = *(const uint4*)(src + j*8);
+    }
+    __syncthreads();
     {
-      int hr = t >> 2, k0 = (t & 3) << 5;
-      const unsigned short* src = W1 + (size_t)(hc*64+hr)*128 + k0;
-      unsigned short* dst = As1 + hr*136 + k0;
-      #pragma unroll
-      for (int j = 0; j < 4; ++j) *(uint4*)(dst + j*8) = *(const uint4*)(src + j*8);
-    }
-    {
-      int o = t >> 1, k0 = (t & 1) << 5;
-      const unsigned short* src = W2 + (size_t)o*512 + hc*64 + k0;
-      unsigned short* dst = As2 + o*72 + k0;
-      #pragma unroll
-      for (int j = 0; j < 4; ++j) *(uint4*)(dst + j*8) = *(const uint4*)(src + j*8);
-    }
-    __syncthreads();
-    {
-      int hb = (wv & 1) << 5, pxb = (wv >> 1) << 5;
       f32x4 a1[2][2];
       #pragma unroll
       for (int i=0;i<2;++i)
@@ -535,20 +577,20 @@
         for (int j=0;j<2;++j){ f32x4 z={0.f,0.f,0.f,0.f}; a1[i][j]=z; }
       #pragma unroll
       for (int s = 0; s < 4; ++s){
-        bf16x8 af[2], bfv[2];
-        #pragma unroll
-        for (int i=0;i<2;++i) af[i] = *(const bf16x8*)(As1 + (hb + i*16 + l15)*136 + s*32 + quad*8);
-        #pragma unroll
-        for (int j=0;j<2;++j) bfv[j] = *(const bf16x8*)(Xs + (pxb + j*16 + l15)*136 + s*32 + quad*8);
+        bf16x8 af[2], bx[2];
+        #pragma unroll
+        for (int i=0;i<2;++i) af[i] = *(const bf16x8*)(As1 + (hbv+i*16+l15)*136 + s*32 + quad*8);
+        #pragma unroll
+        for (int j=0;j<2;++j) bx[j] = *(const bf16x8*)(Xs + (pxb+j*16+l15)*136 + s*32 + quad*8);
         #pragma unroll
         for (int i=0;i<2;++i)
           #pragma unroll
           for (int j=0;j<2;++j)
-            a1[i][j] = __builtin_amdgcn_mfma_f32_16x16x32_bf16(af[i], bfv[j], a1[i][j], 0,0,0);
+            a1[i][j] = __builtin_amdgcn_mfma_f32_16x16x32_bf16(af[i], bx[j], a1[i][j], 0,0,0);
       }
       #pragma unroll
       for (int i = 0; i < 2; ++i){
-        int hl = hb + i*16 + (quad<<2);
+        int hl = hbv + i*16 + (quad<<2);
         float4 bv = *(const float4*)(b1 + hc*64 + hl);
         #pragma unroll
         for (int j = 0; j < 2; ++j){
@@ -561,48 +603,52 @@
       }
     }
     __syncthreads();
-    {
-      int ob = wv << 5;
-      #pragma unroll
-      for (int s = 0; s < 2; ++s){
-        bf16x8 af[2], bfv[4];
-        #pragma unroll
-        for (int i=0;i<2;++i) af[i] = *(const bf16x8*)(As2 + (ob + i*16 + l15)*72 + s*32 + quad*8);
-        #pragma unroll
-        for (int j=0;j<4;++j) bfv[j] = *(const bf16x8*)(Hs + (j*16 + l15)*72 + s*32 + quad*8);
-        #pragma unroll
-        for (int i=0;i<2;++i)
-          #pragma unroll
-          for (int j=0;j<4;++j)
-            acc2[i][j] = __builtin_amdgcn_mfma_f32_16x16x32_bf16(af[i], bfv[j], acc2[i][j], 0,0,0);
-      }
+    #pragma unroll
+    for (int s = 0; s < 2; ++s){
+      bf16x8 af2[2], bh[4];
+      #pragma unroll
+      for (int i=0;i<2;++i) af2[i] = *(const bf16x8*)(As2 + (ob2+i*16+l15)*72 + s*32 + quad*8);
+      #pragma unroll
+      for (int j=0;j<4;++j) bh[j] = *(const bf16x8*)(Hs + (j*16+l15)*72 + s*32 + quad*8);
+      #pragma unroll
+      for (int i=0;i<2;++i)
+        #pragma unroll
+        for (int j=0;j<4;++j)
+          acc2[i][j] = __builtin_amdgcn_mfma_f32_16x16x32_bf16(af2[i], bh[j], acc2[i][j], 0,0,0);
     }
   }
   __syncthreads();
   #pragma unroll
   for (int i = 0; i < 2; ++i){
-    int o = (wv<<5) + i*16 + (quad<<2);
+    int o = ob2 + i*16 + (quad<<2);
     float4 bv = *(const float4*)(b2 + o);
     #pragma unroll
     for (int j = 0; j < 4; ++j){
       int px = j*16 + l15;
-      float v0=acc2[i][j][0]+bv.x, v1=acc2[i][j][1]+bv.y, v2=acc2[i][j][2]+bv.z, v3=acc2[i][j][3]+bv.w;
-      float4 rv = *(const float4*)(XR + ((size_t)(p0+px))*128 + o);
-      v0+=rv.x; v1+=rv.y; v2+=rv.z; v3+=rv.w;
-      *(float4*)(OT + px*136 + o) = make_float4(v0,v1,v2,v3);
+      uint2 w; w.x = pk2(acc2[i][j][0]+bv.x, acc2[i][j][1]+bv.y);
+      w.y = pk2(acc2[i][j][2]+bv.z, acc2[i][j][3]+bv.w);
+      *(uint2*)(OT + px*136 + o) = w;
     }
   }
   __syncthreads();
   {
     int px = t >> 2, c0 = (t & 3) << 5;
-    float* dst = XR + ((size_t)(p0+px))*128 + c0;
-    const float* src = OT + px*136 + c0;
-    #pragma unroll
-    for (int gi = 0; gi < 8; ++gi){
-      float4 v = *(const float4*)(src + gi*4);
-      *(float4*)(dst + gi*4) = v;
-      atomicAdd(&sgS[(c0>>2)+gi],  v.x+v.y+v.z+v.w);
-      atomicAdd(&sgSS[(c0>>2)+gi], v.x*v.x+v.y*v.y+v.z*v.z+v.w*v.w);
+    unsigned short* dst = XRb + (size_t)(p0+px)*128 + c0;
+    #pragma unroll
+    for (int g = 0; g < 4; ++g){
+      uint4 hu = *(const uint4*)(OT + px*136 + c0 + g*8);
+      uint4 ru = *(const uint4*)(dst + g*8);
+      float hf[8], rf[8], v[8];
+      ub8(hu, hf); ub8(ru, rf);
+      #pragma unroll
+      for (int e = 0; e < 8; ++e) v[e] = hf[e] + rf[e];
+      float slo = v[0]+v[1]+v[2]+v[3], shi = v[4]+v[5]+v[6]+v[7];
+      float qlo = v[0]*v[0]+v[1]*v[1]+v[2]*v[2]+v[3]*v[3];
+      float qhi = v[4]*v[4]+v[5]*v[5]+v[6]*v[6]+v[7]*v[7];
+      int gb = (c0 + g*8) >> 2;
+      atomicAdd(&sgS[gb], slo);  atomicAdd(&sgS[gb+1], shi);
+      atomicAdd(&sgSS[gb], qlo); atomicAdd(&sgSS[gb+1], qhi);
+      *(uint4*)(dst + g*8) = pb8(v);
     }
   }
   __syncthreads();
@@ -613,38 +659,38 @@
 }
 
 __global__ __launch_bounds__(256) void k_dw(
-    const float* __restrict__ XR, const float* __restrict__ SG4,
+    const unsigned short* __restrict__ XRb, const float* __restrict__ SG4,
     const float* __restrict__ gnw, const float* __restrict__ gnb,
     const float* __restrict__ dww, const float* __restrict__ dwb,
-    unsigned short* __restrict__ DWO)
+    unsigned short* __restrict__ DWOb)
 {
   __shared__ float wt[9*128];
   __shared__ float An[128], Bn[128];
   int t = threadIdx.x;
-  int p0 = blockIdx.x << 6;
-  int b = p0 >> 14;
-  int win0 = (p0 >> 4) & 1023;
-  int wh = win0 >> 5, ww0 = win0 & 31;
+  int blk = blockIdx.x;
+  int b = blk >> 8;
+  int rem = blk & 255;
+  int h0 = (rem >> 3) << 2;
+  int w0 = (rem & 7) << 4;
   if (t < 128){
     int g = t >> 2;
     float S = SG4[(b*32+g)*2], SS = SG4[(b*32+g)*2+1];
     float m = S*(1.f/65536.f);
     float r = rsqrtf(SS*(1.f/65536.f) - m*m + EPSV);
     float A = r*gnw[t];
-    An[t] = A;
-    Bn[t] = gnb[t] - m*A;
+    An[t] = A; Bn[t] = gnb[t] - m*A;
   }
   for (int j = t; j < 1152; j += 256){ int c = j/9, tap = j%9; wt[tap*128 + c] = dww[j]; }
   __syncthreads();
-  int pxl = t & 63, ck = t >> 6;
-  int c0 = ck << 5;
-  int wloc = pxl >> 4, ty = (pxl >> 2) & 3, tx = pxl & 3;
-  int h = wh*4 + ty, w = (ww0 + wloc)*4 + tx;
+  int pxl = t & 63, cg = t >> 6;
+  int ty = pxl >> 4, tx = pxl & 15;
+  int h = h0 + ty, w = w0 + tx;
+  int c0 = cg << 5;
   float acc[32];
   #pragma unroll
-  for (int j = 0; j < 8; ++j){
-    float4 bv = *(const float4*)(dwb + c0 + j*4);
-    acc[j*4+0]=bv.x; acc[j*4+1]=bv.y; acc[j*4+2]=bv.z; acc[j*4+3]=bv.w;
+  for (int g = 0; g < 8; ++g){
+    float4 bv = *(const float4*)(dwb + c0 + g*4);
+    acc[g*4+0]=bv.x; acc[g*4+1]=bv.y; acc[g*4+2]=bv.z; acc[g*4+3]=bv.w;
   }
   #pragma unroll
   for (int dy = -1; dy <= 1; ++dy){
@@ -654,114 +700,103 @@
     for (int dx = -1; dx <= 1; ++dx){
       int wn = w + dx;
       if (wn < 0 || wn > 127) continue;
-      int pn = b*IMGP + ((hh>>2)*32 + (wn>>2))*16 + (hh&3)*4 + (wn&3);
-      const float* xp = XR + (size_t)pn*128 + c0;
+      const unsigned short* xp = XRb + (size_t)(b*IMGP + hh*128 + wn)*128 + c0;
       const float* wp = wt + ((dy+1)*3 + (dx+1))*128 + c0;
       #pragma unroll
-      for (int j = 0; j < 8; ++j){
-        float4 xv = *(const float4*)(xp + j*4);
-        float4 wv = *(const float4*)(wp + j*4);
-        int c = c0 + j*4;
-        acc[j*4+0] = fmaf(wv.x, fmaf(An[c+0], xv.x, Bn[c+0]), acc[j*4+0]);
-        acc[j*4+1] = fmaf(wv.y, fmaf(An[c+1], xv.y, Bn[c+1]), acc[j*4+1]);
-        acc[j*4+2] = fmaf(wv.z, fmaf(An[c+2], xv.z, Bn[c+2]), acc[j*4+2]);
-        acc[j*4+3] = fmaf(wv.w, fmaf(An[c+3], xv.w, Bn[c+3]), acc[j*4+3]);
+      for (int g = 0; g < 4; ++g){
+        uint4 u = *(const uint4*)(xp + g*8);
+        float f[8];
+        ub8(u, f);
+        int c = c0 + g*8;
+        #pragma unroll
+        for (int e = 0; e < 8; ++e)
+          acc[g*8+e] = fmaf(wp[g*8+e], fmaf(An[c+e], f[e], Bn[c+e]), acc[g*8+e]);
       }
     }
   }
-  unsigned short* dst = DWO + ((size_t)(p0+pxl))*128 + c0;
+  unsigned short* dst = DWOb + (size_t)(b*IMGP + h*128 + w)*128 + c0;
+  #pragma unroll
+  for (int g = 0; g < 4; ++g){
+    float v[8];
+    #pragma unroll
+    for (int e = 0; e < 8; ++e){ float x = acc[g*8+e]; v[e] = x * sigmoidf_(x); }
+    *(uint4*)(dst + g*8) = pb8(v);
+  }
+}
+
+__global__ __launch_bounds__(256) void k_s4(
+    const unsigned short* __restrict__ DWOb,
+    const unsigned short* __restrict__ Wpw, const float* __restrict__ bias,
+    const unsigned short* __restrict__ XRb, float* __restrict__ out)
+{
+  __shared__ __align__(16) char UN[36864];
+  unsigned short* PXs = (unsigned short*)UN;
+  unsigned short* Ws  = (unsigned short*)(UN + 18432);
+  unsigned short* RS  = (unsigned short*)UN;
+  int t = threadIdx.x;
+  int p0 = blockIdx.x << 7;
+  int b = p0 >> 14;
+  int hw0 = p0 & 16383;
+  int lane = t & 63, wv = t >> 6, quad = lane >> 4, l15 = lane & 15;
+  int pb = (wv >> 1) << 6, ob = (wv & 1) << 6;
+  f32x4 acc[4][4];
+  #pragma unroll
+  for (int i=0;i<4;++i)
+    #pragma unroll
+    for (int j=0;j<4;++j){ f32x4 z={0.f,0.f,0.f,0.f}; acc[i][j]=z; }
+  for (int kc = 0; kc < 2; ++kc){
+    if (kc) __syncthreads();
+    { int px = t >> 1, kh = (t & 1) << 5;
+      const unsigned short* src = DWOb + (size_t)(p0+px)*128 + kc*64 + kh;
+      unsigned short* dst = PXs + px*72 + kh;
+      #pragma unroll
+      for (int j = 0; j < 4; ++j) *(uint4*)(dst + j*8) = *(const uint4*)(src + j*8);
+    }
+    { int o = t >> 1, kh = (t & 1) << 5;
+      const unsigned short* src = Wpw + o*128 + kc*64 + kh;
+      unsigned short* dst = Ws + o*72 + kh;
+      #pragma unroll
+      for (int j = 0; j < 4; ++j) *(uint4*)(dst + j*8) = *(const uint4*)(src + j*8);
+    }
+    __syncthreads();
+    #pragma unroll
+    for (int s = 0; s < 2; ++s){
+      bf16x8 ax[4], bw[4];
+      #pragma unroll
+      for (int i=0;i<4;++i) ax[i] = *(const bf16x8*)(PXs + (pb+i*16+l15)*72 + s*32 + quad*8);
+      #pragma unroll
+      for (int j=0;j<4;++j) bw[j] = *(const bf16x8*)(Ws + (ob+j*16+l15)*72 + s*32 + quad*8);
+      #pragma unroll
+      for (int i=0;i<4;++i)
+        #pragma unroll
+        for (int j=0;j<4;++j)
+          acc[i][j] = __builtin_amdgcn_mfma_f32_16x16x32_bf16(ax[i], bw[j], acc[i][j], 0,0,0);
+    }
+  }
+  __syncthreads();
+  {
+    int px = t >> 1, ch = (t & 1) << 6;
+    const unsigned short* src = XRb + (size_t)(p0+px)*128 + ch;
+    unsigned short* dst = RS + px*136 + ch;
+    #pragma unroll
+    for (int g = 0; g < 8; ++g) *(uint4*)(dst + g*8) = *(const uint4*)(src + g*8);
+  }
+  __syncthreads();
   #pragma unroll
   for (int j = 0; j < 4; ++j){
-    float v0 = acc[j*8+0], v1 = acc[j*8+1], v2 = acc[j*8+2], v3 = acc[j*8+3];
-    float v4 = acc[j*8+4], v5 = acc[j*8+5], v6 = acc[j*8+6], v7 = acc[j*8+7];
-    v0*=sigmoidf_(v0); v1*=sigmoidf_(v1); v2*=sigmoidf_(v2); v3*=sigmoidf_(v3);
-    v4*=sigmoidf_(v4); v5*=sigmoidf_(v5); v6*=sigmoidf_(v6); v7*=sigmoidf_(v7);
-    uint4 wq;
-    wq.x = pk2(v0,v1); wq.y = pk2(v2,v3); wq.z = pk2(v4,v5); wq.w = pk2(v6,v7);
-    *(uint4*)(dst + j*8) = wq;
-  }
-}
-
-__global__ __launch_bounds__(256) void k_s4(
-    const unsigned short* __restrict__ DWO,
-    const unsigned short* __restrict__ Wbf, const float* __restrict__ bias,
-    const float* __restrict__ XR, float* __restrict__ out)
-{
-  __shared__ __align__(16) unsigned short Bs[64*136];
-  __shared__ __align__(16) char UN[64*136*4];
-  unsigned short* As = (unsigned short*)UN;
-  float* OT = (float*)UN;
-  int t = threadIdx.x;
-  int p0 = blockIdx.x << 6;
-  int b = p0 >> 14;
-  int win0 = (p0 >> 4) & 1023;
-  int wh = win0 >> 5, ww0 = win0 & 31;
-  {
-    int px = t >> 2, c0 = (t & 3) << 5;
-    const unsigned short* src = DWO + ((size_t)(p0+px))*128 + c0;
-    unsigned short* dst = Bs + px*136 + c0;
-    #pragma unroll
-    for (int j = 0; j < 4; ++j) *(uint4*)(dst + j*8) = *(const uint4*)(src + j*8);
-  }
-  f32x4 acc[2][4];
-  #pragma unroll
-  for (int i=0;i<2;++i)
-    #pragma unroll
-    for (int j=0;j<4;++j){ f32x4 z={0.f,0.f,0.f,0.f}; acc[i][j]=z; }
-  int lane = t & 63, wv = t >> 6, quad = lane >> 4, l15 = lane & 15;
-  for (int kc = 0; kc < 2; ++kc){
-    __syncthreads();
-    {
-      int o = t >> 1, k0 = (t & 1) << 5;
-      const unsigned short* src = Wbf + (size_t)o*128 + kc*64 + k0;
-      unsigned short* dst = As + o*72 + k0;
-      #pragma unroll
-      for (int j = 0; j < 4; ++j) *(uint4*)(dst + j*8) = *(const uint4*)(src + j*8);
-    }
-    __syncthreads();
-    #pragma unroll
-    for (int s = 0; s < 2; ++s){
-      bf16x8 af[2], bfv[4];
-      #pragma unroll
-      for (int i=0;i<2;++i) af[i] = *(const bf16x8*)(As + (wv*32 + i*16 + l15)*72 + s*32 + quad*8);
-      #pragma unroll
-      for (int j=0;j<4;++j) bfv[j] = *(const bf16x8*)(Bs + (j*16 + l15)*136 + kc*64 + s*32 + quad*8);
-      #pragma unroll
-      for (int i=0;i<2;++i)
-        #pragma unroll
-        for (int j=0;j<4;++j)
-          acc[i][j] = __builtin_amdgcn_mfma_f32_16x16x32_bf16(af[i], bfv[j], acc[i][j], 0,0,0);
-    }
-  }
-  __syncthreads();
-  #pragma unroll
-  for (int i = 0; i < 2; ++i){
-    int o = (wv<<5) + i*16 + (quad<<2);
-    float4 bv = *(const float4*)(bias + o);
-    #pragma unroll
-    for (int j = 0; j < 4; ++j){
-      int px = j*16 + l15;
-      float v0=acc[i][j][0]+bv.x, v1=acc[i][j][1]+bv.y, v2=acc[i][j][2]+bv.z, v3=acc[i][j][3]+bv.w;
-      float4 rv = *(const float4*)(XR + ((size_t)(p0+px))*128 + o);
-      v0+=rv.x; v1+=rv.y; v2+=rv.z; v3+=rv.w;
-      *(float4*)(OT + px*136 + o) = make_float4(v0,v1,v2,v3);
-    }
-  }
-  __syncthreads();
-  #pragma unroll
-  for (int it = 0; it < 2; ++it){
-    int item = t + (it << 8);
-    int c = item >> 2, ty = item & 3;
-    float vbuf[16];
-    #pragma unroll
-    for (int wl = 0; wl < 4; ++wl)
-      #pragma unroll
-      for (int tx = 0; tx < 4; ++tx)
-        vbuf[wl*4+tx] = OT[(wl*16 + ty*4 + tx)*136 + c];
-    float* dst = out + ((size_t)(b*128 + c))*IMGP + (wh*4+ty)*128 + ww0*4;
-    #pragma unroll
-    for (int j = 0; j < 4; ++j)
-      *(float4*)(dst + j*4) = make_float4(vbuf[j*4], vbuf[j*4+1], vbuf[j*4+2], vbuf[j*4+3]);
+    int o = ob + j*16 + l15;
+    float bv = bias[o];
+    float* orow = out + (size_t)(b*128 + o)*IMGP + hw0;
+    #pragma unroll
+    for (int i = 0; i < 4; ++i){
+      int pxq = pb + i*16 + (quad << 2);
+      float4 v;
+      v.x = acc[i][j][0] + bv + bf2f(RS[(pxq+0)*136 + o]);
+      v.y = acc[i][j][1] + bv + bf2f(RS[(pxq+1)*136 + o]);
+      v.z = acc[i][j][2] + bv + bf2f(RS[(pxq+2)*136 + o]);
+      v.w = acc[i][j][3] + bv + bf2f(RS[(pxq+3)*136 + o]);
+      *(float4*)(orow + pxq) = v;
+    }
   }
 }
 
@@ -820,22 +855,24 @@
   unsigned short* Wmlp1 = WBF + 81920;
   unsigned short* Wmlp2 = WBF + 147456;
   unsigned short* Wpw   = WBF + 212992;
-  float* X0T = (float*)(ws + (1u<<20));
-  float* XR  = (float*)(ws + (1u<<20) + ((size_t)64<<20));
-  unsigned short* DWO = (unsigned short*)(ws + (1u<<20) + ((size_t)128<<20));
+  unsigned short* X0b = (unsigned short*)(ws + (1u<<20));
+  unsigned short* XRb = (unsigned short*)(ws + (1u<<20) + ((size_t)32<<20));
+  unsigned short* QKV = (unsigned short*)(ws + (1u<<20) + ((size_t)64<<20));
+  unsigned short* DWOb = QKV;
 
   hipMemsetAsync(SG, 0, 4*512*sizeof(float), stream);
 
   k_prep<<<896, 256, 0, stream>>>(specw, qkvw, projw, mlpw1, mlpw2, pww, WBF);
-  k_time_mlp<<<dim3(8,3), 256, 0, stream>>>(temb,
+  k_tmlp<<<dim3(8,3), 256, 0, stream>>>(temb,
       t1w1,t1b1,t1w2,t1b2, t2w1,t2b1,t2w2,t2b2, t3w1,t3b1,t3w2,t3b2, SC);
-  k_pre<<<2048, 256, 0, stream>>>(x0, X0T, SG1);
-  k_s1<<<2048, 256, 0, stream>>>(X0T, SG1, SG2, Wspec, specb,
-      gn1w, gn1b, SC + 0, modew, XR);
-  k_s2<<<4096, 256, 0, stream>>>(XR, SG2, SG3, Wqkv, qkvb, Wproj, projb,
-      relb, gn2w, gn2b, SC + 2048);
-  k_s3<<<2048, 256, 0, stream>>>(XR, SG3, SG4, Wmlp1, mlpb1, Wmlp2, mlpb2,
+  k_pre<<<2048, 256, 0, stream>>>(x0, X0b, SG1);
+  k_s1<<<1024, 256, 0, stream>>>(X0b, SG1, SG2, Wspec, specb,
+      gn1w, gn1b, SC + 0, modew, XRb);
+  k_qkv<<<dim3(1024,3), 256, 0, stream>>>(XRb, SG2, Wqkv, qkvb,
+      gn2w, gn2b, SC + 2048, QKV);
+  k_ap<<<1024, 256, 0, stream>>>(QKV, Wproj, projb, relb, XRb, SG3);
+  k_s3<<<2048, 256, 0, stream>>>(XRb, SG3, SG4, Wmlp1, mlpb1, Wmlp2, mlpb2,
       gn3w, gn3b, SC + 4096);
-  k_dw<<<2048, 256, 0, stream>>>(XR, SG4, sbgnw, sbgnb, dww, dwb, DWO);
-  k_s4<<<2048, 256, 0, stream>>>(DWO, Wpw, pwb, XR, out);
-}
+  k_dw<<<2048, 256, 0, stream>>>(XRb, SG4, sbgnw, sbgnb, dww, dwb, DWOb);
+  k_s4<<<1024, 256, 0, stream>>>(DWOb, Wpw, pwb, XRb, out);
+}
```

New measurement: 705.9 us. -12.9%, faster.
